# Kernel tuning notes

Hardware: AMD Instinct MI355X
Metric: run time of the kernel (lower is better)

## Reference

```python
import jax, jax.numpy as jnp
import numpy as np

B, L, D = 4, 1024, 256
HD = 16                 # head_dim
H = D // HD             # num heads = 16
DI = 2 * D              # mamba d_inner (expand=2) = 512
S = 64                  # d_state
KC = 4                  # d_conv
DTR = max(1, D // 16)   # dt_rank = 16
SCALES = (1, 2, 4, 8)


def _lin_interp(x, L_out):
    # F.interpolate(mode='linear', align_corners=False) on (B, L_in, D)
    L_in = x.shape[1]
    pos = (jnp.arange(L_out, dtype=x.dtype) + 0.5) * (L_in / L_out) - 0.5
    pos = jnp.clip(pos, 0.0, L_in - 1)
    lo = jnp.floor(pos).astype(jnp.int32)
    hi = jnp.minimum(lo + 1, L_in - 1)
    w = (pos - lo.astype(x.dtype))[None, :, None]
    return x[:, lo] * (1.0 - w) + x[:, hi] * w


def setup_inputs() -> dict:
    key = jax.random.key(0)
    ks = jax.random.split(key, 24)
    sc = 0.02
    inp = {
        "x": jax.random.normal(ks[0], (B, L, D), jnp.float32),
        "ln_g": jnp.ones((D,), jnp.float32),
        "ln_b": jnp.zeros((D,), jnp.float32),
        # MultiScaleQuery: 4 per-scale projections + fuse
        "mq_w": sc * jax.random.normal(ks[1], (4, D, D), jnp.float32),
        "mq_b": sc * jax.random.normal(ks[2], (4, D), jnp.float32),
        "fuse_w": sc * jax.random.normal(ks[3], (D, 4 * D), jnp.float32),
        "fuse_b": sc * jax.random.normal(ks[4], (D,), jnp.float32),
        # Mamba params
        "in_proj_w": sc * jax.random.normal(ks[5], (2 * DI, D), jnp.float32),
        "conv_w": 0.2 * jax.random.normal(ks[6], (DI, KC), jnp.float32),
        "conv_b": sc * jax.random.normal(ks[7], (DI,), jnp.float32),
        "x_proj_w": sc * jax.random.normal(ks[8], (DTR + 2 * S, DI), jnp.float32),
        "dt_w": sc * jax.random.normal(ks[9], (DI, DTR), jnp.float32),
        "dt_b": jnp.full((DI,), -4.0, jnp.float32),  # softplus -> small dt
        "A_log": jnp.log(jnp.tile(jnp.arange(1, S + 1, dtype=jnp.float32), (DI, 1))),
        "D_ssm": jnp.ones((DI,), jnp.float32),
        "out_w": sc * jax.random.normal(ks[10], (D, DI), jnp.float32),
        # StructuredSSD (q comes from MultiScaleQuery override; q_proj unused)
        "k_w": sc * jax.random.normal(ks[11], (D, D), jnp.float32),
        "k_b": sc * jax.random.normal(ks[12], (D,), jnp.float32),
        "v_w": sc * jax.random.normal(ks[13], (D, D), jnp.float32),
        "v_b": sc * jax.random.normal(ks[14], (D,), jnp.float32),
        "o_w": sc * jax.random.normal(ks[15], (D, D), jnp.float32),
        "o_b": sc * jax.random.normal(ks[16], (D,), jnp.float32),
        "log_tau": jnp.full((H,), np.log(16.0), jnp.float32),
        # Gate
        "gate_w": sc * jax.random.normal(ks[17], (D, 2 * D), jnp.float32),
        "gate_b": sc * jax.random.normal(ks[18], (D,), jnp.float32),
    }
    return inp


def reference(x, ln_g, ln_b, mq_w, mq_b, fuse_w, fuse_b,
              in_proj_w, conv_w, conv_b, x_proj_w, dt_w, dt_b,
              A_log, D_ssm, out_w,
              k_w, k_b, v_w, v_b, o_w, o_b, log_tau,
              gate_w, gate_b):
    Bsz, Lq, Dm = x.shape

    # ---- LayerNorm ----
    mu = x.mean(-1, keepdims=True)
    var = ((x - mu) ** 2).mean(-1, keepdims=True)
    xn = (x - mu) / jnp.sqrt(var + 1e-5) * ln_g + ln_b

    # ---- MultiScaleQuery ----
    qs = []
    for i, s in enumerate(SCALES):
        if s <= 1:
            q = xn @ mq_w[i].T + mq_b[i]
        else:
            xd = xn.reshape(Bsz, Lq // s, s, Dm).mean(2)   # avg_pool1d(k=s, stride=s)
            qd = xd @ mq_w[i].T + mq_b[i]
            q = _lin_interp(qd, Lq)
        qs.append(q)
    q = jnp.concatenate(qs, -1) @ fuse_w.T + fuse_b        # (B, L, D)

    # ---- Mamba (selective scan) ----
    xz = xn @ in_proj_w.T                                  # (B, L, 2*DI)
    xm, z = jnp.split(xz, 2, axis=-1)
    xp = jnp.pad(xm, ((0, 0), (KC - 1, 0), (0, 0)))        # causal depthwise conv
    xc = sum(xp[:, kk:kk + Lq, :] * conv_w[:, kk] for kk in range(KC)) + conv_b
    xc = jax.nn.silu(xc)                                   # (B, L, DI)
    dbc = xc @ x_proj_w.T                                  # (B, L, DTR+2S)
    dt_in, Bm, Cm = jnp.split(dbc, [DTR, DTR + S], axis=-1)
    dt = jax.nn.softplus(dt_in @ dt_w.T + dt_b)            # (B, L, DI)
    A = -jnp.exp(A_log)                                    # (DI, S)

    def step(h, inp):
        xt, dtt, Bt, Ct = inp                              # (B,DI) (B,DI) (B,S) (B,S)
        dA = jnp.exp(dtt[:, :, None] * A)                  # (B, DI, S)
        h = dA * h + (dtt * xt)[:, :, None] * Bt[:, None, :]
        y = jnp.einsum('bds,bs->bd', h, Ct)
        return h, y

    h0 = jnp.zeros((Bsz, DI, S), x.dtype)
    _, ys = jax.lax.scan(step, h0, (xc.transpose(1, 0, 2), dt.transpose(1, 0, 2),
                                    Bm.transpose(1, 0, 2), Cm.transpose(1, 0, 2)))
    y = ys.transpose(1, 0, 2) + xc * D_ssm                 # (B, L, DI)
    y = y * jax.nn.silu(z)
    ssm_out = y @ out_w.T                                  # (B, L, D)

    # ---- StructuredSSD (decay-masked attention, q override) ----
    k = xn @ k_w.T + k_b
    v = xn @ v_w.T + v_b
    hds = lambda t: t.reshape(Bsz, Lq, H, HD).transpose(0, 2, 1, 3)
    qh, kh, vh = hds(q), hds(k), hds(v)                    # (B, H, L, hd)
    scale = 1.0 / np.sqrt(HD)
    scores = jnp.einsum('bhqd,bhkd->bhqk', qh, kh) * scale
    idx = jnp.arange(Lq)
    dist = jnp.maximum(idx[:, None] - idx[None, :], 0).astype(x.dtype)
    tau = jnp.exp(log_tau)[:, None, None]                  # (H,1,1)
    mask = jnp.exp(-dist / tau)                            # (H, L, L); ==1 above diag
    scores = scores * mask
    denom = jnp.maximum(mask.sum(-1, keepdims=True), 1e-6)
    scores = scores / denom                                # broadcast over batch
    attn = jnp.einsum('bhqk,bhkd->bhqd', scores, vh)
    attn = attn.transpose(0, 2, 1, 3).reshape(Bsz, Lq, Dm)
    ssd_out = attn @ o_w.T + o_b

    # ---- Sigmoid gate fusion + residual ----
    gate = jax.nn.sigmoid(jnp.concatenate([ssm_out, ssd_out], -1) @ gate_w.T + gate_b)
    fused = gate * ssm_out + (1.0 - gate) * ssd_out
    return x + fused
```

## Files before the change

kernel.cpp:

```cpp
#include <hip/hip_runtime.h>
#include <math.h>

#define Bsz 4
#define Lseq 1024
#define Dm 256
#define Hh 16
#define HDm 16
#define DIm 512
#define Ssz 64
#define KCm 4
#define DTRm 16
#define NCH (Bsz * DIm)
#define CHK 64
#define NCHK (Lseq / CHK)
#define CHA 16
#define NCA (Lseq / CHA)

typedef __attribute__((ext_vector_type(8))) short s8v;
typedef __attribute__((ext_vector_type(4))) short s4v;
typedef __attribute__((ext_vector_type(4))) float f4v;
typedef unsigned short u16;

static __device__ __forceinline__ float wave_sum(float v) {
    #pragma unroll
    for (int m = 32; m >= 1; m >>= 1) v += __shfl_xor(v, m, 64);
    return v;
}

static __device__ __forceinline__ float bcast(float v, int l) {
    return __uint_as_float(__builtin_amdgcn_readlane(__float_as_uint(v), l));
}

static __device__ __forceinline__ short f2bf(float f) {
    unsigned int u = __float_as_uint(f);
    u = (u + 0x7fffu + ((u >> 16) & 1u)) >> 16;
    return (short)u;
}

static __device__ __forceinline__ float bf2f(u16 u) {
    return __uint_as_float(((unsigned int)u) << 16);
}

static __device__ __forceinline__ s8v pack8(float4 a, float4 b) {
    s8v v;
    v[0] = f2bf(a.x); v[1] = f2bf(a.y); v[2] = f2bf(a.z); v[3] = f2bf(a.w);
    v[4] = f2bf(b.x); v[5] = f2bf(b.y); v[6] = f2bf(b.z); v[7] = f2bf(b.w);
    return v;
}

static __device__ __forceinline__ s4v pack4(float4 a) {
    s4v v;
    v[0] = f2bf(a.x); v[1] = f2bf(a.y); v[2] = f2bf(a.z); v[3] = f2bf(a.w);
    return v;
}

__global__ __launch_bounds__(256) void ln_pool(const float* __restrict__ x,
                                               const float* __restrict__ g,
                                               const float* __restrict__ bb,
                                               u16* __restrict__ xnb, u16* __restrict__ xd2b,
                                               u16* __restrict__ xd4b, u16* __restrict__ xd8b,
                                               const float* __restrict__ in_proj_w,
                                               const float* __restrict__ k_w,
                                               const float* __restrict__ v_w,
                                               const float* __restrict__ mq_w,
                                               const float* __restrict__ fuse_w,
                                               const float* __restrict__ x_proj_w,
                                               const float* __restrict__ out_w,
                                               const float* __restrict__ o_w,
                                               const float* __restrict__ gate_w,
                                               u16* __restrict__ wbf) {
    int bx = blockIdx.x;
    int tid = threadIdx.x;
    if (bx < 512) {
        __shared__ float p2[4][256];
        int wid = tid >> 6, lane = tid & 63;
        int gr0 = bx * 8;
        int b = gr0 >> 10, t0 = gr0 & 1023;
        float4 g4 = *(const float4*)(g + lane * 4);
        float4 b4 = *(const float4*)(bb + lane * 4);
        float4 res[2];
        #pragma unroll
        for (int rr = 0; rr < 2; rr++) {
            int row = gr0 + wid * 2 + rr;
            float4 xv = *(const float4*)(x + (size_t)row * 256 + lane * 4);
            float s = wave_sum(xv.x + xv.y + xv.z + xv.w);
            float mean = s * (1.0f / 256.0f);
            float d0 = xv.x - mean, d1 = xv.y - mean, d2 = xv.z - mean, d3 = xv.w - mean;
            float s2 = wave_sum(d0 * d0 + d1 * d1 + d2 * d2 + d3 * d3);
            float inv = rsqrtf(s2 * (1.0f / 256.0f) + 1e-5f);
            float4 r;
            r.x = d0 * inv * g4.x + b4.x; r.y = d1 * inv * g4.y + b4.y;
            r.z = d2 * inv * g4.z + b4.z; r.w = d3 * inv * g4.w + b4.w;
            *(s4v*)(xnb + (size_t)row * 256 + lane * 4) = pack4(r);
            res[rr] = r;
        }
        float4 a2;
        a2.x = 0.5f * (res[0].x + res[1].x); a2.y = 0.5f * (res[0].y + res[1].y);
        a2.z = 0.5f * (res[0].z + res[1].z); a2.w = 0.5f * (res[0].w + res[1].w);
        *(s4v*)(xd2b + (size_t)(b * 512 + (t0 >> 1) + wid) * 256 + lane * 4) = pack4(a2);
        *(float4*)&p2[wid][lane * 4] = a2;
        __syncthreads();
        if (wid < 2) {
            float4 u = *(const float4*)&p2[2 * wid][lane * 4];
            float4 w = *(const float4*)&p2[2 * wid + 1][lane * 4];
            float4 m;
            m.x = 0.5f * (u.x + w.x); m.y = 0.5f * (u.y + w.y);
            m.z = 0.5f * (u.z + w.z); m.w = 0.5f * (u.w + w.w);
            *(s4v*)(xd4b + (size_t)(b * 256 + (t0 >> 2) + wid) * 256 + lane * 4) = pack4(m);
        } else if (wid == 2) {
            float4 q0 = *(const float4*)&p2[0][lane * 4];
            float4 q1 = *(const float4*)&p2[1][lane * 4];
            float4 q2 = *(const float4*)&p2[2][lane * 4];
            float4 q3 = *(const float4*)&p2[3][lane * 4];
            float4 m;
            m.x = 0.25f * ((q0.x + q1.x) + (q2.x + q3.x));
            m.y = 0.25f * ((q0.y + q1.y) + (q2.y + q3.y));
            m.z = 0.25f * ((q0.z + q1.z) + (q2.z + q3.z));
            m.w = 0.25f * ((q0.w + q1.w) + (q2.w + q3.w));
            *(s4v*)(xd8b + (size_t)(b * 128 + (t0 >> 3)) * 256 + lane * 4) = pack4(m);
        }
    } else {
        int l = bx - 512;
        const float* src; u16* dst; int base;
        if (l < 128)      { src = in_proj_w; dst = wbf;           base = l; }
        else if (l < 160) { src = k_w;      dst = wbf + 262144;   base = l - 128; }
        else if (l < 192) { src = v_w;      dst = wbf + 327680;   base = l - 160; }
        else if (l < 320) { src = mq_w;     dst = wbf + 393216;   base = l - 192; }
        else if (l < 448) { src = fuse_w;   dst = wbf + 655360;   base = l - 320; }
        else if (l < 484) { src = x_proj_w; dst = wbf + 917504;   base = l - 448; }
        else if (l < 548) { src = out_w;    dst = wbf + 991232;   base = l - 484; }
        else if (l < 580) { src = o_w;      dst = wbf + 1122304;  base = l - 548; }
        else              { src = gate_w;   dst = wbf + 1187840;  base = l - 580; }
        int idx = base * 2048 + tid * 8;
        const float* sp = src + idx;
        *(s8v*)(dst + idx) = pack8(*(const float4*)sp, *(const float4*)(sp + 4));
    }
}

__global__ __launch_bounds__(256) void proj8(const u16* __restrict__ xnb,
                                             const u16* __restrict__ xd2b,
                                             const u16* __restrict__ xd4b,
                                             const u16* __restrict__ xd8b,
                                             const u16* __restrict__ wbf,
                                             const float* __restrict__ k_b,
                                             const float* __restrict__ v_b,
                                             const float* __restrict__ mq_b,
                                             u16* __restrict__ xmb, float* __restrict__ zT,
                                             float* __restrict__ kmat, float* __restrict__ vmat,
                                             u16* __restrict__ q0b, u16* __restrict__ qd2b,
                                             u16* __restrict__ qd4b, u16* __restrict__ qd8b) {
    __shared__ u16 As[64][40];
    __shared__ u16 Ws[64][40];
    int bx = blockIdx.x;
    const u16* A; const u16* W; const float* bias;
    float* Cf = nullptr; u16* Cb = nullptr;
    int ldc, transC = 0, n0, m0;
    if (bx < 512) {
        A = xnb; W = wbf; bias = nullptr; Cb = xmb; ldc = DIm;
        n0 = (bx & 7) * 64; m0 = (bx >> 3) * 64;
    } else if (bx < 1024) {
        int l = bx - 512;
        A = xnb; W = wbf + 131072; bias = nullptr; Cf = zT; ldc = Bsz * Lseq; transC = 1;
        n0 = (l & 7) * 64; m0 = (l >> 3) * 64;
    } else if (bx < 1280) {
        int l = bx - 1024;
        A = xnb; W = wbf + 262144; bias = k_b; Cf = kmat; ldc = Dm;
        n0 = (l & 3) * 64; m0 = (l >> 2) * 64;
    } else if (bx < 1536) {
        int l = bx - 1280;
        A = xnb; W = wbf + 327680; bias = v_b; Cf = vmat; ldc = Dm;
        n0 = (l & 3) * 64; m0 = (l >> 2) * 64;
    } else if (bx < 1792) {
        int l = bx - 1536;
        A = xnb; W = wbf + 393216; bias = mq_b; Cb = q0b; ldc = Dm;
        n0 = (l & 3) * 64; m0 = (l >> 2) * 64;
    } else if (bx < 1920) {
        int l = bx - 1792;
        A = xd2b; W = wbf + 393216 + 65536; bias = mq_b + 256; Cb = qd2b; ldc = Dm;
        n0 = (l & 3) * 64; m0 = (l >> 2) * 64;
    } else if (bx < 1984) {
        int l = bx - 1920;
        A = xd4b; W = wbf + 393216 + 131072; bias = mq_b + 512; Cb = qd4b; ldc = Dm;
        n0 = (l & 3) * 64; m0 = (l >> 2) * 64;
    } else {
        int l = bx - 1984;
        A = xd8b; W = wbf + 393216 + 196608; bias = mq_b + 768; Cb = qd8b; ldc = Dm;
        n0 = (l & 3) * 64; m0 = (l >> 2) * 64;
    }
    int tid = threadIdx.x;
    int wave = tid >> 6, lane = tid & 63;
    int quad = lane >> 4, r = lane & 15;
    int mo = (wave >> 1) * 32, no = (wave & 1) * 32;
    f4v acc[2][2];
    #pragma unroll
    for (int i = 0; i < 2; i++)
        #pragma unroll
        for (int j = 0; j < 2; j++) acc[i][j] = (f4v){0.f, 0.f, 0.f, 0.f};
    for (int k0 = 0; k0 < 256; k0 += 32) {
        {
            int m = tid >> 2, kk = (tid & 3) * 8;
            *(s8v*)&As[m][kk] = *(const s8v*)(A + (size_t)(m0 + m) * 256 + k0 + kk);
        }
        {
            int n = tid >> 2, kk = (tid & 3) * 8;
            *(s8v*)&Ws[n][kk] = *(const s8v*)(W + (size_t)(n0 + n) * 256 + k0 + kk);
        }
        __syncthreads();
        s8v af[2], bf[2];
        #pragma unroll
        for (int i = 0; i < 2; i++) af[i] = *(const s8v*)&As[mo + i * 16 + r][quad * 8];
        #pragma unroll
        for (int j = 0; j < 2; j++) bf[j] = *(const s8v*)&Ws[no + j * 16 + r][quad * 8];
        #pragma unroll
        for (int i = 0; i < 2; i++)
            #pragma unroll
            for (int j = 0; j < 2; j++)
                acc[i][j] = __builtin_amdgcn_mfma_f32_16x16x32_bf16(af[i], bf[j], acc[i][j], 0, 0, 0);
        __syncthreads();
    }
    #pragma unroll
    for (int i = 0; i < 2; i++)
        #pragma unroll
        for (int j = 0; j < 2; j++)
            #pragma unroll
            for (int reg = 0; reg < 4; reg++) {
                int m = m0 + mo + i * 16 + quad * 4 + reg;
                int n = n0 + no + j * 16 + r;
                float v = acc[i][j][reg];
                if (bias) v += bias[n];
                if (Cb) Cb[(size_t)m * ldc + n] = (u16)f2bf(v);
                else {
                    float* cp = transC ? (Cf + (size_t)n * ldc + m) : (Cf + (size_t)m * ldc + n);
                    *cp = v;
                }
            }
}

__global__ __launch_bounds__(256) void mid2(const u16* __restrict__ q0b,
                                            const u16* __restrict__ qd2b,
                                            const u16* __restrict__ qd4b,
                                            const u16* __restrict__ qd8b,
                                            const u16* __restrict__ w_fuse,
                                            const float* __restrict__ fuse_b,
                                            float* __restrict__ qbuf,
                                            const u16* __restrict__ xmb,
                                            const float* __restrict__ cw,
                                            const float* __restrict__ cb,
                                            u16* __restrict__ xcb, float* __restrict__ xcT) {
    __shared__ __align__(16) char smem[16640];
    int bx = blockIdx.x;
    int tid = threadIdx.x;
    if (bx < 256) {
        u16 (*As)[40] = (u16(*)[40])smem;
        u16 (*Ws)[40] = (u16(*)[40])(smem + 5120);
        int wave = tid >> 6, lane = tid & 63;
        int quad = lane >> 4, r = lane & 15;
        int n0 = (bx & 3) * 64, m0 = (bx >> 2) * 64;
        int mo = (wave >> 1) * 32, no = (wave & 1) * 32;
        f4v acc[2][2];
        #pragma unroll
        for (int i = 0; i < 2; i++)
            #pragma unroll
            for (int j = 0; j < 2; j++) acc[i][j] = (f4v){0.f, 0.f, 0.f, 0.f};
        for (int k0 = 0; k0 < 1024; k0 += 32) {
            {
                int m = tid >> 2, kk = (tid & 3) * 8;
                int kg = k0 + kk;
                int seg = kg >> 8, dcol = kg & 255;
                int mg = m0 + m;
                s8v pv;
                if (seg == 0) {
                    pv = *(const s8v*)(q0b + (size_t)mg * 256 + dcol);
                } else {
                    int t = mg & 1023, b = mg >> 10;
                    int Lin = 512 >> (seg - 1);
                    const u16* qd = (seg == 1) ? qd2b : (seg == 2) ? qd4b : qd8b;
                    float pos = (t + 0.5f) * ((float)Lin / 1024.0f) - 0.5f;
                    pos = fminf(fmaxf(pos, 0.0f), (float)(Lin - 1));
                    int lo = (int)floorf(pos);
                    int hi = min(lo + 1, Lin - 1);
                    float w = pos - (float)lo;
                    s8v lv = *(const s8v*)(qd + ((size_t)(b * Lin + lo)) * 256 + dcol);
                    s8v hv = *(const s8v*)(qd + ((size_t)(b * Lin + hi)) * 256 + dcol);
                    #pragma unroll
                    for (int i = 0; i < 8; i++) {
                        float lf = bf2f((u16)lv[i]), hf = bf2f((u16)hv[i]);
                        pv[i] = f2bf(lf + w * (hf - lf));
                    }
                }
                *(s8v*)&As[m][kk] = pv;
            }
            {
                int n = tid >> 2, kk = (tid & 3) * 8;
                *(s8v*)&Ws[n][kk] = *(const s8v*)(w_fuse + (size_t)(n0 + n) * 1024 + k0 + kk);
            }
            __syncthreads();
            s8v af[2], bf[2];
            #pragma unroll
            for (int i = 0; i < 2; i++) af[i] = *(const s8v*)&As[mo + i * 16 + r][quad * 8];
            #pragma unroll
            for (int j = 0; j < 2; j++) bf[j] = *(const s8v*)&Ws[no + j * 16 + r][quad * 8];
            #pragma unroll
            for (int i = 0; i < 2; i++)
                #pragma unroll
                for (int j = 0; j < 2; j++)
                    acc[i][j] = __builtin_amdgcn_mfma_f32_16x16x32_bf16(af[i], bf[j], acc[i][j], 0, 0, 0);
            __syncthreads();
        }
        #pragma unroll
        for (int i = 0; i < 2; i++)
            #pragma unroll
            for (int j = 0; j < 2; j++)
                #pragma unroll
                for (int reg = 0; reg < 4; reg++) {
                    int m = m0 + mo + i * 16 + quad * 4 + reg;
                    int n = n0 + no + j * 16 + r;
                    qbuf[(size_t)m * 256 + n] = acc[i][j][reg] + fuse_b[n];
                }
    } else {
        float (*tile)[65] = (float(*)[65])smem;
        int blk = bx - 256;
        int cblk = blk & 7;
        int tblk = (blk >> 3) & 15;
        int b = blk >> 7;
        int c0 = cblk * 64, t0 = tblk * 64;
        int cc = tid & 63;
        int tw = tid >> 6;
        int c = c0 + cc;
        float w0 = cw[c * 4 + 0], w1 = cw[c * 4 + 1], w2 = cw[c * 4 + 2], w3 = cw[c * 4 + 3];
        float bias = cb[c];
        #pragma unroll 4
        for (int i = 0; i < 16; i++) {
            int tl = tw * 16 + i;
            int t = t0 + tl;
            const u16* base = xmb + ((size_t)(b * Lseq + t)) * DIm + c;
            float acc = bias + bf2f(base[0]) * w3;
            if (t >= 3) {
                acc += bf2f(base[-3 * DIm]) * w0 + bf2f(base[-2 * DIm]) * w1 + bf2f(base[-1 * DIm]) * w2;
            } else {
                if (t >= 1) acc += bf2f(base[-1 * DIm]) * w2;
                if (t >= 2) acc += bf2f(base[-2 * DIm]) * w1;
            }
            float r = acc / (1.0f + __expf(-acc));
            xcb[((size_t)(b * Lseq + t)) * DIm + c] = (u16)f2bf(r);
            tile[tl][cc] = r;
        }
        __syncthreads();
        int tcol = tid & 63;
        int crow0 = tid >> 6;
        #pragma unroll 4
        for (int j = 0; j < 16; j++) {
            int crow = crow0 * 16 + j;
            xcT[((size_t)(c0 + crow)) * (Bsz * Lseq) + b * Lseq + t0 + tcol] = tile[tcol][crow];
        }
    }
}

__global__ __launch_bounds__(256) void xproj_ap1(const u16* __restrict__ xcb,
                                                 const u16* __restrict__ w_xp,
                                                 float* __restrict__ dbc,
                                                 const float* __restrict__ kmat,
                                                 const float* __restrict__ vmat,
                                                 const float* __restrict__ log_tau,
                                                 float* __restrict__ loc) {
    __shared__ __align__(16) char smem[10240];
    int bx = blockIdx.x;
    int tid = threadIdx.x;
    int wid = tid >> 6, lane = tid & 63;
    if (bx < 192) {
        u16 (*As)[40] = (u16(*)[40])smem;
        u16 (*Ws)[40] = (u16(*)[40])(smem + 5120);
        int quad = lane >> 4, r = lane & 15;
        int n0 = (bx % 3) * 64, m0 = (bx / 3) * 64;
        int mo = (wid >> 1) * 32, no = (wid & 1) * 32;
        f4v acc[2][2];
        #pragma unroll
        for (int i = 0; i < 2; i++)
            #pragma unroll
            for (int j = 0; j < 2; j++) acc[i][j] = (f4v){0.f, 0.f, 0.f, 0.f};
        for (int k0 = 0; k0 < 512; k0 += 32) {
            {
                int m = tid >> 2, kk = (tid & 3) * 8;
                *(s8v*)&As[m][kk] = *(const s8v*)(xcb + (size_t)(m0 + m) * 512 + k0 + kk);
            }
            {
                int n = tid >> 2, kk = (tid & 3) * 8;
                s8v pv;
                if (n0 + n < 144) pv = *(const s8v*)(w_xp + (size_t)(n0 + n) * 512 + k0 + kk);
                else pv = (s8v){0, 0, 0, 0, 0, 0, 0, 0};
                *(s8v*)&Ws[n][kk] = pv;
            }
            __syncthreads();
            s8v af[2], bf[2];
            #pragma unroll
            for (int i = 0; i < 2; i++) af[i] = *(const s8v*)&As[mo + i * 16 + r][quad * 8];
            #pragma unroll
            for (int j = 0; j < 2; j++) bf[j] = *(const s8v*)&Ws[no + j * 16 + r][quad * 8];
            #pragma unroll
            for (int i = 0; i < 2; i++)
                #pragma unroll
                for (int j = 0; j < 2; j++)
                    acc[i][j] = __builtin_amdgcn_mfma_f32_16x16x32_bf16(af[i], bf[j], acc[i][j], 0, 0, 0);
            __syncthreads();
        }
        #pragma unroll
        for (int i = 0; i < 2; i++)
            #pragma unroll
            for (int j = 0; j < 2; j++)
                #pragma unroll
                for (int reg = 0; reg < 4; reg++) {
                    int m = m0 + mo + i * 16 + quad * 4 + reg;
                    int n = n0 + no + j * 16 + r;
                    if (n >= 144) continue;
                    dbc[(size_t)m * 144 + n] = acc[i][j][reg];
                }
    } else {
        float (*Ksh)[CHA][20] = (float(*)[CHA][20])smem;
        float (*Vsh)[CHA][16] = (float(*)[CHA][16])(smem + 5120);
        int wv = (bx - 192) * 4 + wid;
        int bh = wv >> 6, c = wv & 63;
        int b = bh >> 4, h = bh & 15;
        float inv_tau = __expf(-log_tau[h]);
        float rdec = __expf(-inv_tau);
        int t0 = c * CHA;
        int row = lane >> 2, q4 = (lane & 3) * 4;
        const float* kp = kmat + ((size_t)(b * Lseq + t0 + row)) * Dm + h * HDm + q4;
        const float* vp = vmat + ((size_t)(b * Lseq + t0 + row)) * Dm + h * HDm + q4;
        *(float4*)&Ksh[wid][row][q4] = *(const float4*)kp;
        *(float4*)&Vsh[wid][row][q4] = *(const float4*)vp;
        int g = lane >> 4, cc = lane & 15;
        float4 U = {0.f, 0.f, 0.f, 0.f}, T = {0.f, 0.f, 0.f, 0.f};
        #pragma unroll
        for (int s = 0; s < CHA; s++) {
            float4 kf = *(const float4*)&Ksh[wid][s][4 * g];
            float vv = Vsh[wid][s][cc];
            float u0 = kf.x * vv, u1 = kf.y * vv, u2 = kf.z * vv, u3 = kf.w * vv;
            U.x += u0; U.y += u1; U.z += u2; U.w += u3;
            T.x = fmaf(rdec, T.x, u0); T.y = fmaf(rdec, T.y, u1);
            T.z = fmaf(rdec, T.z, u2); T.w = fmaf(rdec, T.w, u3);
        }
        float* op = loc + ((size_t)bh * NCA + c) * 512;
        *(float4*)(op + lane * 4) = U;
        *(float4*)(op + 256 + lane * 4) = T;
    }
}

__global__ __launch_bounds__(256) void dt_ap2(const float* __restrict__ dbc,
                                              const float* __restrict__ dt_w,
                                              const float* __restrict__ dt_b,
                                              float* __restrict__ dtmT,
                                              float* __restrict__ loc,
                                              const float* __restrict__ log_tau,
                                              float* __restrict__ kvtot) {
    __shared__ __align__(16) char smem[9216];
    int bx = blockIdx.x;
    int tid = threadIdx.x;
    if (bx < 512) {
        float (*As)[72] = (float(*)[72])smem;
        float (*Ws)[72] = (float(*)[72])(smem + 4608);
        int m0 = (bx >> 3) * 64, n0 = (bx & 7) * 64;
        int tx = tid & 15, ty = tid >> 4;
        float acc[4][4] = {};
        {
            int ml = tid >> 2, kl = (tid & 3) * 4;
            const float4 av = *(const float4*)(dbc + (size_t)(m0 + ml) * 144 + kl);
            As[kl + 0][ml] = av.x; As[kl + 1][ml] = av.y;
            As[kl + 2][ml] = av.z; As[kl + 3][ml] = av.w;
        }
        {
            int nl = tid >> 2, kl = (tid & 3) * 4;
            float4 wv = *(const float4*)(dt_w + (size_t)(n0 + nl) * 16 + kl);
            Ws[kl + 0][nl] = wv.x; Ws[kl + 1][nl] = wv.y;
            Ws[kl + 2][nl] = wv.z; Ws[kl + 3][nl] = wv.w;
        }
        __syncthreads();
        #pragma unroll
        for (int kk = 0; kk < 16; kk++) {
            float4 av = *(const float4*)&As[kk][ty * 4];
            float4 bv = *(const float4*)&Ws[kk][tx * 4];
            float a[4] = {av.x, av.y, av.z, av.w};
            float bbv[4] = {bv.x, bv.y, bv.z, bv.w};
            #pragma unroll
            for (int im = 0; im < 4; im++)
                #pragma unroll
                for (int in = 0; in < 4; in++)
                    acc[im][in] = fmaf(a[im], bbv[in], acc[im][in]);
        }
        #pragma unroll
        for (int in = 0; in < 4; in++) {
            int n = n0 + tx * 4 + in;
            #pragma unroll
            for (int im = 0; im < 4; im++) {
                int m = m0 + ty * 4 + im;
                float v = acc[im][in] + dt_b[n];
                v = fmaxf(v, 0.0f) + log1pf(expf(-fabsf(v)));
                dtmT[(size_t)n * (Bsz * Lseq) + m] = v;
            }
        }
    } else {
        int bh = bx - 512, e = tid;
        float inv_tau = __expf(-log_tau[bh & 15]);
        float rp = __expf(-(float)CHA * inv_tau);
        float* lp = loc + (size_t)bh * NCA * 512;
        float Ua = 0.f, Ta = 0.f;
        #pragma unroll 8
        for (int c = 0; c < NCA; c++) {
            float tu = lp[c * 512 + e];
            lp[c * 512 + e] = Ua;
            Ua += tu;
            float tt = lp[c * 512 + 256 + e];
            lp[c * 512 + 256 + e] = Ta;
            Ta = fmaf(rp, Ta, tt);
        }
        kvtot[bh * 256 + e] = Ua;
    }
}

__global__ __launch_bounds__(256) void sp1_ap3(const float* __restrict__ xcT,
                                               const float* __restrict__ dtmT,
                                               const float* __restrict__ dbc,
                                               const float* __restrict__ A_log,
                                               float* __restrict__ hloc,
                                               float* __restrict__ Pc,
                                               const float* __restrict__ q,
                                               const float* __restrict__ kmat,
                                               const float* __restrict__ vmat,
                                               const float* __restrict__ log_tau,
                                               const float* __restrict__ init,
                                               const float* __restrict__ kvtot,
                                               u16* __restrict__ attnb) {
    __shared__ __align__(16) char smem[18432];
    int bx = blockIdx.x;
    int tid = threadIdx.x;
    int wid = tid >> 6, lane = tid & 63;
    if (bx < 8192) {
        int wave = bx * 4 + wid;
        int ch = wave & (NCH - 1);
        int c  = wave >> 11;
        int b = ch >> 9, d = ch & (DIm - 1);
        float As = -__expf(A_log[d * Ssz + lane]);
        int base_m = b * Lseq + c * CHK;
        float dt_vec = dtmT[(size_t)d * (Bsz * Lseq) + base_m + lane];
        float x_vec  = xcT [(size_t)d * (Bsz * Lseq) + base_m + lane];
        float ux = dt_vec * x_vec;
        float S = dt_vec;
        #pragma unroll
        for (int m = 1; m < 64; m <<= 1) {
            float o = __shfl_up(S, m, 64);
            if (lane >= m) S += o;
        }
        float Stot = bcast(S, 63);
        const float* Bp = dbc + (size_t)base_m * 144 + DTRm + lane;
        float h0 = 0.f, h1 = 0.f, h2 = 0.f, h3 = 0.f;
        #pragma unroll 4
        for (int t = 0; t < CHK; t += 4) {
            float B0 = Bp[0], B1 = Bp[144], B2 = Bp[288], B3 = Bp[432];
            Bp += 576;
            float w0 = __expf(As * (Stot - bcast(S, t)))     * bcast(ux, t);
            float w1 = __expf(As * (Stot - bcast(S, t + 1))) * bcast(ux, t + 1);
            float w2 = __expf(As * (Stot - bcast(S, t + 2))) * bcast(ux, t + 2);
            float w3 = __expf(As * (Stot - bcast(S, t + 3))) * bcast(ux, t + 3);
            h0 = fmaf(w0, B0, h0); h1 = fmaf(w1, B1, h1);
            h2 = fmaf(w2, B2, h2); h3 = fmaf(w3, B3, h3);
        }
        size_t o = ((size_t)ch * NCHK + c) * Ssz + lane;
        hloc[o] = (h0 + h1) + (h2 + h3);
        Pc[o] = __expf(As * Stot);
    } else {
        float (*Ksh)[CHA][20] = (float(*)[CHA][20])smem;
        float (*Qsh)[CHA][20] = (float(*)[CHA][20])(smem + 5120);
        float (*Vsh)[CHA][16] = (float(*)[CHA][16])(smem + 10240);
        float (*Ysh)[CHA][16] = (float(*)[CHA][16])(smem + 14336);
        int wv = (bx - 8192) * 4 + wid;
        int bh = wv >> 6, c = wv & 63;
        int b = bh >> 4, h = bh & 15;
        float inv_tau = __expf(-log_tau[h]);
        float rdec = __expf(-inv_tau);
        int t0 = c * CHA;
        int row = lane >> 2, q4 = (lane & 3) * 4;
        const float* kp = kmat + ((size_t)(b * Lseq + t0 + row)) * Dm + h * HDm + q4;
        const float* vp = vmat + ((size_t)(b * Lseq + t0 + row)) * Dm + h * HDm + q4;
        const float* qp = q    + ((size_t)(b * Lseq + t0 + row)) * Dm + h * HDm + q4;
        *(float4*)&Ksh[wid][row][q4] = *(const float4*)kp;
        *(float4*)&Vsh[wid][row][q4] = *(const float4*)vp;
        *(float4*)&Qsh[wid][row][q4] = *(const float4*)qp;
        int g = lane >> 4, cc = lane & 15;
        size_t ibase = ((size_t)bh * NCA + c) * 512;
        float4 U  = *(const float4*)(init + ibase + lane * 4);
        float4 T  = *(const float4*)(init + ibase + 256 + lane * 4);
        float4 KV = *(const float4*)(kvtot + bh * 256 + lane * 4);
        float om = 1.0f - rdec;
        float geom = (om > 1e-8f) ? (1.0f - __expf(-inv_tau * (float)t0)) / om : (float)t0;
        #pragma unroll
        for (int s = 0; s < CHA; s++) {
            int i = t0 + s;
            geom = fmaf(geom, rdec, 1.0f);
            float4 kf = *(const float4*)&Ksh[wid][s][4 * g];
            float4 qf = *(const float4*)&Qsh[wid][s][4 * g];
            float vv = Vsh[wid][s][cc];
            float u0 = kf.x * vv, u1 = kf.y * vv, u2 = kf.z * vv, u3 = kf.w * vv;
            U.x += u0; U.y += u1; U.z += u2; U.w += u3;
            T.x = fmaf(rdec, T.x, u0); T.y = fmaf(rdec, T.y, u1);
            T.z = fmaf(rdec, T.z, u2); T.w = fmaf(rdec, T.w, u3);
            float p;
            p = qf.x * (KV.x - U.x + T.x);
            p = fmaf(qf.y, KV.y - U.y + T.y, p);
            p = fmaf(qf.z, KV.z - U.z + T.z, p);
            p = fmaf(qf.w, KV.w - U.w + T.w, p);
            p += __shfl_xor(p, 16, 64);
            p += __shfl_xor(p, 32, 64);
            float deno = fmaxf((float)(Lseq - 1 - i) + geom, 1e-6f);
            float yv = p * (0.25f / deno);
            if (lane < 16) Ysh[wid][s][lane] = yv;
        }
        float4 yv4 = *(const float4*)&Ysh[wid][row][q4];
        *(s4v*)(attnb + ((size_t)(b * Lseq + t0 + row)) * Dm + h * HDm + q4) = pack4(yv4);
    }
}

__global__ __launch_bounds__(256) void comb_ssd(float* __restrict__ hloc,
                                                const float* __restrict__ Pc,
                                                const u16* __restrict__ attnb,
                                                const u16* __restrict__ w_o,
                                                const float* __restrict__ o_b,
                                                u16* __restrict__ cat2b) {
    __shared__ u16 As[64][40];
    __shared__ u16 Ws[64][40];
    int bx = blockIdx.x;
    int tid = threadIdx.x;
    if (bx < 512) {
        int wave = bx * 4 + (tid >> 6);
        int lane = tid & 63;
        size_t base = (size_t)wave * NCHK * Ssz + lane;
        float H = 0.0f;
        #pragma unroll
        for (int c = 0; c < NCHK; c++) {
            size_t o = base + (size_t)c * Ssz;
            float p = Pc[o];
            float hl = hloc[o];
            hloc[o] = H;
            H = fmaf(p, H, hl);
        }
    } else {
        int l = bx - 512;
        int wave = tid >> 6, lane = tid & 63;
        int quad = lane >> 4, r = lane & 15;
        int n0 = (l & 3) * 64, m0 = (l >> 2) * 64;
        int mo = (wave >> 1) * 32, no = (wave & 1) * 32;
        f4v acc[2][2];
        #pragma unroll
        for (int i = 0; i < 2; i++)
            #pragma unroll
            for (int j = 0; j < 2; j++) acc[i][j] = (f4v){0.f, 0.f, 0.f, 0.f};
        for (int k0 = 0; k0 < 256; k0 += 32) {
            {
                int m = tid >> 2, kk = (tid & 3) * 8;
                *(s8v*)&As[m][kk] = *(const s8v*)(attnb + (size_t)(m0 + m) * 256 + k0 + kk);
            }
            {
                int n = tid >> 2, kk = (tid & 3) * 8;
                *(s8v*)&Ws[n][kk] = *(const s8v*)(w_o + (size_t)(n0 + n) * 256 + k0 + kk);
            }
            __syncthreads();
            s8v af[2], bf[2];
            #pragma unroll
            for (int i = 0; i < 2; i++) af[i] = *(const s8v*)&As[mo + i * 16 + r][quad * 8];
            #pragma unroll
            for (int j = 0; j < 2; j++) bf[j] = *(const s8v*)&Ws[no + j * 16 + r][quad * 8];
            #pragma unroll
            for (int i = 0; i < 2; i++)
                #pragma unroll
                for (int j = 0; j < 2; j++)
                    acc[i][j] = __builtin_amdgcn_mfma_f32_16x16x32_bf16(af[i], bf[j], acc[i][j], 0, 0, 0);
            __syncthreads();
        }
        #pragma unroll
        for (int i = 0; i < 2; i++)
            #pragma unroll
            for (int j = 0; j < 2; j++)
                #pragma unroll
                for (int reg = 0; reg < 4; reg++) {
                    int m = m0 + mo + i * 16 + quad * 4 + reg;
                    int n = n0 + no + j * 16 + r;
                    cat2b[(size_t)m * 512 + 256 + n] = (u16)f2bf(acc[i][j][reg] + o_b[n]);
                }
    }
}

__global__ __launch_bounds__(256) void scan_pass3(const float* __restrict__ xcT,
                                                  const float* __restrict__ dtmT,
                                                  const float* __restrict__ zT,
                                                  const float* __restrict__ dbc,
                                                  const float* __restrict__ A_log,
                                                  const float* __restrict__ D_ssm,
                                                  const float* __restrict__ Hinit,
                                                  u16* __restrict__ yTb) {
    __shared__ float hCs[4][16][68];
    int wid = threadIdx.x >> 6;
    int lane = threadIdx.x & 63;
    int wave = blockIdx.x * 4 + wid;
    int ch = wave & (NCH - 1);
    int c  = wave >> 11;
    int b = ch >> 9, d = ch & (DIm - 1);
    float As = -__expf(A_log[d * Ssz + lane]);
    float Dd = D_ssm[d];
    int base_m = b * Lseq + c * CHK;
    float dt_vec = dtmT[(size_t)d * (Bsz * Lseq) + base_m + lane];
    float x_vec  = xcT [(size_t)d * (Bsz * Lseq) + base_m + lane];
    float zown   = zT  [(size_t)d * (Bsz * Lseq) + base_m + lane];
    float ux = dt_vec * x_vec;
    const float* Bp = dbc + (size_t)base_m * 144 + DTRm + lane;
    const float* Cp = Bp + Ssz;
    float h = Hinit[((size_t)ch * NCHK + c) * Ssz + lane];
    float yred = 0.0f;
    int tl = lane >> 2;
    int so = (lane & 3) * 16;
    for (int tb = 0; tb < 4; tb++) {
        #pragma unroll
        for (int j = 0; j < 16; j++) {
            int t = tb * 16 + j;
            float Bt = *Bp; Bp += 144;
            float Ct = *Cp; Cp += 144;
            float dtv = bcast(dt_vec, t);
            float u   = bcast(ux, t);
            float dA = __expf(dtv * As);
            h = fmaf(dA, h, u * Bt);
            hCs[wid][j][lane] = h * Ct;
        }
        const float* bp = &hCs[wid][tl][so];
        float4 a0 = *(const float4*)(bp + 0);
        float4 a1 = *(const float4*)(bp + 4);
        float4 a2 = *(const float4*)(bp + 8);
        float4 a3 = *(const float4*)(bp + 12);
        float part = ((a0.x + a0.y) + (a0.z + a0.w)) + ((a1.x + a1.y) + (a1.z + a1.w))
                   + ((a2.x + a2.y) + (a2.z + a2.w)) + ((a3.x + a3.y) + (a3.z + a3.w));
        part += __shfl_xor(part, 1, 64);
        part += __shfl_xor(part, 2, 64);
        float got = __shfl(part, ((lane - tb * 16) << 2) & 63, 64);
        if ((lane >> 4) == tb) yred = got;
    }
    float yg = (yred + x_vec * Dd) * (zown / (1.0f + __expf(-zown)));
    yTb[(size_t)d * (Bsz * Lseq) + base_m + lane] = (u16)f2bf(yg);
}

__global__ __launch_bounds__(256) void outg(const u16* __restrict__ yTb,
                                            const u16* __restrict__ w_out,
                                            u16* __restrict__ cat2b) {
    __shared__ u16 As[64][40];
    __shared__ u16 Ws[64][40];
    int bx = blockIdx.x;
    int tid = threadIdx.x;
    int wave = tid >> 6, lane = tid & 63;
    int quad = lane >> 4, r = lane & 15;
    int n0 = (bx & 3) * 64, m0 = (bx >> 2) * 64;
    int mo = (wave >> 1) * 32, no = (wave & 1) * 32;
    f4v acc[2][2];
    #pragma unroll
    for (int i = 0; i < 2; i++)
        #pragma unroll
        for (int j = 0; j < 2; j++) acc[i][j] = (f4v){0.f, 0.f, 0.f, 0.f};
    for (int k0 = 0; k0 < 512; k0 += 32) {
        {
            int k = tid >> 3, m8 = (tid & 7) * 8;
            s8v av = *(const s8v*)(yTb + (size_t)(k0 + k) * (Bsz * Lseq) + m0 + m8);
            #pragma unroll
            for (int i = 0; i < 8; i++) As[m8 + i][k] = (u16)av[i];
        }
        {
            int n = tid >> 2, kk = (tid & 3) * 8;
            *(s8v*)&Ws[n][kk] = *(const s8v*)(w_out + (size_t)(n0 + n) * 512 + k0 + kk);
        }
        __syncthreads();
        s8v af[2], bf[2];
        #pragma unroll
        for (int i = 0; i < 2; i++) af[i] = *(const s8v*)&As[mo + i * 16 + r][quad * 8];
        #pragma unroll
        for (int j = 0; j < 2; j++) bf[j] = *(const s8v*)&Ws[no + j * 16 + r][quad * 8];
        #pragma unroll
        for (int i = 0; i < 2; i++)
            #pragma unroll
            for (int j = 0; j < 2; j++)
                acc[i][j] = __builtin_amdgcn_mfma_f32_16x16x32_bf16(af[i], bf[j], acc[i][j], 0, 0, 0);
        __syncthreads();
    }
    #pragma unroll
    for (int i = 0; i < 2; i++)
        #pragma unroll
        for (int j = 0; j < 2; j++)
            #pragma unroll
            for (int reg = 0; reg < 4; reg++) {
                int m = m0 + mo + i * 16 + quad * 4 + reg;
                int n = n0 + no + j * 16 + r;
                cat2b[(size_t)m * 512 + n] = (u16)f2bf(acc[i][j][reg]);
            }
}

__global__ __launch_bounds__(256) void gate_gemm(const u16* __restrict__ cat2b,
                                                 const u16* __restrict__ w_gate,
                                                 const float* __restrict__ gate_b,
                                                 const float* __restrict__ xres,
                                                 float* __restrict__ fout) {
    __shared__ u16 As[64][40];
    __shared__ u16 Ws[64][40];
    int tid = threadIdx.x;
    int wave = tid >> 6, lane = tid & 63;
    int quad = lane >> 4, r = lane & 15;
    int m0 = blockIdx.y * 64, n0 = blockIdx.x * 64;
    int mo = (wave >> 1) * 32, no = (wave & 1) * 32;
    f4v acc[2][2];
    #pragma unroll
    for (int i = 0; i < 2; i++)
        #pragma unroll
        for (int j = 0; j < 2; j++) acc[i][j] = (f4v){0.f, 0.f, 0.f, 0.f};
    for (int k0 = 0; k0 < 512; k0 += 32) {
        {
            int m = tid >> 2, kk = (tid & 3) * 8;
            *(s8v*)&As[m][kk] = *(const s8v*)(cat2b + (size_t)(m0 + m) * 512 + k0 + kk);
        }
        {
            int n = tid >> 2, kk = (tid & 3) * 8;
            *(s8v*)&Ws[n][kk] = *(const s8v*)(w_gate + (size_t)(n0 + n) * 512 + k0 + kk);
        }
        __syncthreads();
        s8v af[2], bf[2];
        #pragma unroll
        for (int i = 0; i < 2; i++) af[i] = *(const s8v*)&As[mo + i * 16 + r][quad * 8];
        #pragma unroll
        for (int j = 0; j < 2; j++) bf[j] = *(const s8v*)&Ws[no + j * 16 + r][quad * 8];
        #pragma unroll
        for (int i = 0; i < 2; i++)
            #pragma unroll
            for (int j = 0; j < 2; j++)
                acc[i][j] = __builtin_amdgcn_mfma_f32_16x16x32_bf16(af[i], bf[j], acc[i][j], 0, 0, 0);
        __syncthreads();
    }
    #pragma unroll
    for (int i = 0; i < 2; i++)
        #pragma unroll
        for (int j = 0; j < 2; j++)
            #pragma unroll
            for (int reg = 0; reg < 4; reg++) {
                int m = m0 + mo + i * 16 + quad * 4 + reg;
                int n = n0 + no + j * 16 + r;
                float v = acc[i][j][reg] + gate_b[n];
                float gg = 1.0f / (1.0f + __expf(-v));
                float ssm = bf2f(cat2b[(size_t)m * 512 + n]);
                float ssd = bf2f(cat2b[(size_t)m * 512 + 256 + n]);
                fout[(size_t)m * 256 + n] = xres[(size_t)m * 256 + n] + gg * ssm + (1.0f - gg) * ssd;
            }
}

extern "C" void kernel_launch(void* const* d_in, const int* in_sizes, int n_in,
                              void* d_out, int out_size, void* d_ws, size_t ws_size,
                              hipStream_t stream) {
    const float* x        = (const float*)d_in[0];
    const float* ln_g     = (const float*)d_in[1];
    const float* ln_b     = (const float*)d_in[2];
    const float* mq_w     = (const float*)d_in[3];
    const float* mq_b     = (const float*)d_in[4];
    const float* fuse_w   = (const float*)d_in[5];
    const float* fuse_b   = (const float*)d_in[6];
    const float* in_proj_w= (const float*)d_in[7];
    const float* conv_w   = (const float*)d_in[8];
    const float* conv_b   = (const float*)d_in[9];
    const float* x_proj_w = (const float*)d_in[10];
    const float* dt_w     = (const float*)d_in[11];
    const float* dt_b     = (const float*)d_in[12];
    const float* A_log    = (const float*)d_in[13];
    const float* D_ssm    = (const float*)d_in[14];
    const float* out_w    = (const float*)d_in[15];
    const float* k_w      = (const float*)d_in[16];
    const float* k_b      = (const float*)d_in[17];
    const float* v_w      = (const float*)d_in[18];
    const float* v_b      = (const float*)d_in[19];
    const float* o_w      = (const float*)d_in[20];
    const float* o_b      = (const float*)d_in[21];
    const float* log_tau  = (const float*)d_in[22];
    const float* gate_w   = (const float*)d_in[23];
    const float* gate_b   = (const float*)d_in[24];
    float* outp = (float*)d_out;

    const int M = Bsz * Lseq;
    float* ws = (float*)d_ws;
    size_t off = 0;
    float* zT    = ws + off; off += (size_t)DIm * M;
    float* xcT   = ws + off; off += (size_t)DIm * M;
    float* dtmT  = ws + off; off += (size_t)DIm * M;
    float* dbc   = ws + off; off += (size_t)M * 144;
    float* qbuf  = ws + off; off += (size_t)M * Dm;
    float* kmat  = ws + off; off += (size_t)M * Dm;
    float* vmat  = ws + off; off += (size_t)M * Dm;
    float* loc   = ws + off; off += (size_t)64 * NCA * 512;
    float* hloc  = ws + off; off += (size_t)NCH * NCHK * Ssz;
    float* Pc    = ws + off; off += (size_t)NCH * NCHK * Ssz;
    float* kvtot = ws + off; off += (size_t)64 * 256;
    u16* ub = (u16*)(ws + off);
    size_t uo = 0;
    u16* xnb  = ub + uo; uo += (size_t)M * Dm;
    u16* xmb  = ub + uo; uo += (size_t)M * DIm;
    u16* xd2b = ub + uo; uo += (size_t)2048 * Dm;
    u16* xd4b = ub + uo; uo += (size_t)1024 * Dm;
    u16* xd8b = ub + uo; uo += (size_t)512 * Dm;
    u16* q0b  = ub + uo; uo += (size_t)M * Dm;
    u16* qd2b = ub + uo; uo += (size_t)2048 * Dm;
    u16* qd4b = ub + uo; uo += (size_t)1024 * Dm;
    u16* qd8b = ub + uo; uo += (size_t)512 * Dm;
    u16* attnb= ub + uo; uo += (size_t)M * Dm;
    u16* cat2b= ub + uo; uo += (size_t)M * 2 * Dm;
    u16* yTb  = ub + uo; uo += (size_t)DIm * M;
    u16* wbf  = ub + uo; uo += 1318912;
    u16* xcb  = cat2b;

    ln_pool<<<1156, 256, 0, stream>>>(x, ln_g, ln_b, xnb, xd2b, xd4b, xd8b,
        in_proj_w, k_w, v_w, mq_w, fuse_w, x_proj_w, out_w, o_w, gate_w, wbf);

    proj8<<<2016, 256, 0, stream>>>(xnb, xd2b, xd4b, xd8b, wbf,
        k_b, v_b, mq_b, xmb, zT, kmat, vmat, q0b, qd2b, qd4b, qd8b);

    mid2<<<768, 256, 0, stream>>>(q0b, qd2b, qd4b, qd8b, wbf + 655360, fuse_b, qbuf,
        xmb, conv_w, conv_b, xcb, xcT);

    xproj_ap1<<<1216, 256, 0, stream>>>(xcb, wbf + 917504, dbc, kmat, vmat, log_tau, loc);

    dt_ap2<<<576, 256, 0, stream>>>(dbc, dt_w, dt_b, dtmT, loc, log_tau, kvtot);

    sp1_ap3<<<9216, 256, 0, stream>>>(xcT, dtmT, dbc, A_log, hloc, Pc,
        qbuf, kmat, vmat, log_tau, loc, kvtot, attnb);

    comb_ssd<<<768, 256, 0, stream>>>(hloc, Pc, attnb, wbf + 1122304, o_b, cat2b);

    scan_pass3<<<8192, 256, 0, stream>>>(xcT, dtmT, zT, dbc, A_log, D_ssm, hloc, yTb);

    outg<<<256, 256, 0, stream>>>(yTb, wbf + 991232, cat2b);

    gate_gemm<<<dim3(4, 64), 256, 0, stream>>>(cat2b, wbf + 1187840, gate_b, x, outp);
}
```

Before: 294.2 us.

## Fold dt projection into weights and restructure kernel chain with precomputed gate weights

Precomputes the combined dt_w·x_proj weight and the product of the gate weight with the out-projection weight in the prep kernel. dt is then computed directly by one bf16 MFMA GEMM with fused softplus, and the gate pre-activation is split into two GEMM partial sums plus a separate elementwise final kernel. Stages are regrouped into fewer, differently fused launches (sp1_ap2, comb_ap3, p3_og, outg_gpre, final_k), and a shared MFMA core helper replaces the duplicated loops. The aim is fewer launches and less fp32 dt work. The cost is extra bf16 rounding of the folded weights and additional fp32 intermediate buffers.

```diff
diff --git a/kernel.cpp b/kernel.cpp
--- a/kernel.cpp
+++ b/kernel.cpp
@@ -8,13 +8,13 @@
 #define HDm 16
 #define DIm 512
 #define Ssz 64
-#define KCm 4
 #define DTRm 16
 #define NCH (Bsz * DIm)
 #define CHK 64
 #define NCHK (Lseq / CHK)
 #define CHA 16
 #define NCA (Lseq / CHA)
+#define LOG2E 1.44269504088896f
 
 typedef __attribute__((ext_vector_type(8))) short s8v;
 typedef __attribute__((ext_vector_type(4))) short s4v;
@@ -53,6 +53,51 @@
     v[0] = f2bf(a.x); v[1] = f2bf(a.y); v[2] = f2bf(a.z); v[3] = f2bf(a.w);
     return v;
 }
+
+static __device__ __forceinline__ void mfma_core(const u16* __restrict__ A, int lda,
+                                                 const u16* __restrict__ W, int ldw,
+                                                 int m0, int n0, int K,
+                                                 u16 (*As)[40], u16 (*Ws)[40],
+                                                 f4v acc[2][2], int tid) {
+    int wave = tid >> 6, lane = tid & 63;
+    int quad = lane >> 4, r = lane & 15;
+    int mo = (wave >> 1) * 32, no = (wave & 1) * 32;
+    for (int k0 = 0; k0 < K; k0 += 32) {
+        {
+            int m = tid >> 2, kk = (tid & 3) * 8;
+            *(s8v*)&As[m][kk] = *(const s8v*)(A + (size_t)(m0 + m) * lda + k0 + kk);
+        }
+        {
+            int n = tid >> 2, kk = (tid & 3) * 8;
+            *(s8v*)&Ws[n][kk] = *(const s8v*)(W + (size_t)(n0 + n) * ldw + k0 + kk);
+        }
+        __syncthreads();
+        s8v af[2], bf[2];
+        #pragma unroll
+        for (int i = 0; i < 2; i++) af[i] = *(const s8v*)&As[mo + i * 16 + r][quad * 8];
+        #pragma unroll
+        for (int j = 0; j < 2; j++) bf[j] = *(const s8v*)&Ws[no + j * 16 + r][quad * 8];
+        #pragma unroll
+        for (int i = 0; i < 2; i++)
+            #pragma unroll
+            for (int j = 0; j < 2; j++)
+                acc[i][j] = __builtin_amdgcn_mfma_f32_16x16x32_bf16(af[i], bf[j], acc[i][j], 0, 0, 0);
+        __syncthreads();
+    }
+}
+
+#define WB_INPJ 0
+#define WB_K    262144
+#define WB_V    327680
+#define WB_MQ   393216
+#define WB_FUSE 655360
+#define WB_XP   917504
+#define WB_OUT  991232
+#define WB_O    1122304
+#define WB_GATE 1187840
+#define WB_OUTT 1318912
+#define WB_WDT  1449984
+#define WB_W1P  1712128
 
 __global__ __launch_bounds__(256) void ln_pool(const float* __restrict__ x,
                                                const float* __restrict__ g,
@@ -68,6 +113,7 @@
                                                const float* __restrict__ out_w,
                                                const float* __restrict__ o_w,
                                                const float* __restrict__ gate_w,
+                                               const float* __restrict__ dt_w,
                                                u16* __restrict__ wbf) {
     int bx = blockIdx.x;
     int tid = threadIdx.x;
@@ -119,21 +165,44 @@
             m.w = 0.25f * ((q0.w + q1.w) + (q2.w + q3.w));
             *(s4v*)(xd8b + (size_t)(b * 128 + (t0 >> 3)) * 256 + lane * 4) = pack4(m);
         }
-    } else {
+    } else if (bx < 1156) {
         int l = bx - 512;
         const float* src; u16* dst; int base;
-        if (l < 128)      { src = in_proj_w; dst = wbf;           base = l; }
-        else if (l < 160) { src = k_w;      dst = wbf + 262144;   base = l - 128; }
-        else if (l < 192) { src = v_w;      dst = wbf + 327680;   base = l - 160; }
-        else if (l < 320) { src = mq_w;     dst = wbf + 393216;   base = l - 192; }
-        else if (l < 448) { src = fuse_w;   dst = wbf + 655360;   base = l - 320; }
-        else if (l < 484) { src = x_proj_w; dst = wbf + 917504;   base = l - 448; }
-        else if (l < 548) { src = out_w;    dst = wbf + 991232;   base = l - 484; }
-        else if (l < 580) { src = o_w;      dst = wbf + 1122304;  base = l - 548; }
-        else              { src = gate_w;   dst = wbf + 1187840;  base = l - 580; }
+        if (l < 128)      { src = in_proj_w; dst = wbf + WB_INPJ; base = l; }
+        else if (l < 160) { src = k_w;      dst = wbf + WB_K;    base = l - 128; }
+        else if (l < 192) { src = v_w;      dst = wbf + WB_V;    base = l - 160; }
+        else if (l < 320) { src = mq_w;     dst = wbf + WB_MQ;   base = l - 192; }
+        else if (l < 448) { src = fuse_w;   dst = wbf + WB_FUSE; base = l - 320; }
+        else if (l < 484) { src = x_proj_w; dst = wbf + WB_XP;   base = l - 448; }
+        else if (l < 548) { src = out_w;    dst = wbf + WB_OUT;  base = l - 484; }
+        else if (l < 580) { src = o_w;      dst = wbf + WB_O;    base = l - 548; }
+        else              { src = gate_w;   dst = wbf + WB_GATE; base = l - 580; }
         int idx = base * 2048 + tid * 8;
         const float* sp = src + idx;
         *(s8v*)(dst + idx) = pack8(*(const float4*)sp, *(const float4*)(sp + 4));
+    } else if (bx < 1412) {
+        int l = bx - 1156;
+        int gid = l * 1024 + tid * 4;
+        int n = gid >> 9, d0 = gid & 511;
+        float4 acc = {0.f, 0.f, 0.f, 0.f};
+        #pragma unroll
+        for (int k = 0; k < 16; k++) {
+            float wv = dt_w[n * 16 + k];
+            float4 xp = *(const float4*)(x_proj_w + (size_t)k * 512 + d0);
+            acc.x = fmaf(wv, xp.x, acc.x); acc.y = fmaf(wv, xp.y, acc.y);
+            acc.z = fmaf(wv, xp.z, acc.z); acc.w = fmaf(wv, xp.w, acc.w);
+        }
+        *(s4v*)(wbf + WB_WDT + (size_t)n * 512 + d0) = pack4(acc);
+    } else {
+        int l = bx - 1412;
+        int gid = l * 2048 + tid * 8;
+        int k = gid >> 9, d0 = gid & 511;
+        float4 a0 = *(const float4*)(out_w + (size_t)k * 512 + d0);
+        float4 a1 = *(const float4*)(out_w + (size_t)k * 512 + d0 + 4);
+        float vv[8] = {a0.x, a0.y, a0.z, a0.w, a1.x, a1.y, a1.z, a1.w};
+        #pragma unroll
+        for (int i = 0; i < 8; i++)
+            wbf[WB_OUTT + (size_t)(d0 + i) * 256 + k] = (u16)f2bf(vv[i]);
     }
 }
 
@@ -141,7 +210,7 @@
                                              const u16* __restrict__ xd2b,
                                              const u16* __restrict__ xd4b,
                                              const u16* __restrict__ xd8b,
-                                             const u16* __restrict__ wbf,
+                                             u16* __restrict__ wbf,
                                              const float* __restrict__ k_b,
                                              const float* __restrict__ v_b,
                                              const float* __restrict__ mq_b,
@@ -152,72 +221,59 @@
     __shared__ u16 As[64][40];
     __shared__ u16 Ws[64][40];
     int bx = blockIdx.x;
+    int tid = threadIdx.x;
     const u16* A; const u16* W; const float* bias;
     float* Cf = nullptr; u16* Cb = nullptr;
-    int ldc, transC = 0, n0, m0;
+    int lda, ldw, ldc, K = 256, n0, m0;
     if (bx < 512) {
-        A = xnb; W = wbf; bias = nullptr; Cb = xmb; ldc = DIm;
+        A = xnb; lda = 256; W = wbf + WB_INPJ; ldw = 256; bias = nullptr; Cb = xmb; ldc = DIm;
         n0 = (bx & 7) * 64; m0 = (bx >> 3) * 64;
     } else if (bx < 1024) {
         int l = bx - 512;
-        A = xnb; W = wbf + 131072; bias = nullptr; Cf = zT; ldc = Bsz * Lseq; transC = 1;
-        n0 = (l & 7) * 64; m0 = (l >> 3) * 64;
+        A = wbf + WB_INPJ + 131072; lda = 256; W = xnb; ldw = 256; bias = nullptr;
+        Cf = zT; ldc = 4096;
+        m0 = (l >> 6) * 64; n0 = (l & 63) * 64;
     } else if (bx < 1280) {
         int l = bx - 1024;
-        A = xnb; W = wbf + 262144; bias = k_b; Cf = kmat; ldc = Dm;
+        A = xnb; lda = 256; W = wbf + WB_K; ldw = 256; bias = k_b; Cf = kmat; ldc = Dm;
         n0 = (l & 3) * 64; m0 = (l >> 2) * 64;
     } else if (bx < 1536) {
         int l = bx - 1280;
-        A = xnb; W = wbf + 327680; bias = v_b; Cf = vmat; ldc = Dm;
+        A = xnb; lda = 256; W = wbf + WB_V; ldw = 256; bias = v_b; Cf = vmat; ldc = Dm;
         n0 = (l & 3) * 64; m0 = (l >> 2) * 64;
     } else if (bx < 1792) {
         int l = bx - 1536;
-        A = xnb; W = wbf + 393216; bias = mq_b; Cb = q0b; ldc = Dm;
+        A = xnb; lda = 256; W = wbf + WB_MQ; ldw = 256; bias = mq_b; Cb = q0b; ldc = Dm;
         n0 = (l & 3) * 64; m0 = (l >> 2) * 64;
     } else if (bx < 1920) {
         int l = bx - 1792;
-        A = xd2b; W = wbf + 393216 + 65536; bias = mq_b + 256; Cb = qd2b; ldc = Dm;
+        A = xd2b; lda = 256; W = wbf + WB_MQ + 65536; ldw = 256; bias = mq_b + 256; Cb = qd2b; ldc = Dm;
         n0 = (l & 3) * 64; m0 = (l >> 2) * 64;
     } else if (bx < 1984) {
         int l = bx - 1920;
-        A = xd4b; W = wbf + 393216 + 131072; bias = mq_b + 512; Cb = qd4b; ldc = Dm;
+        A = xd4b; lda = 256; W = wbf + WB_MQ + 131072; ldw = 256; bias = mq_b + 512; Cb = qd4b; ldc = Dm;
         n0 = (l & 3) * 64; m0 = (l >> 2) * 64;
     } else {
-        int l = bx - 1984;
-        A = xd8b; W = wbf + 393216 + 196608; bias = mq_b + 768; Cb = qd8b; ldc = Dm;
-        n0 = (l & 3) * 64; m0 = (l >> 2) * 64;
+        if (bx < 2016) {
+            int l = bx - 1984;
+            A = xd8b; lda = 256; W = wbf + WB_MQ + 196608; ldw = 256; bias = mq_b + 768; Cb = qd8b; ldc = Dm;
+            n0 = (l & 3) * 64; m0 = (l >> 2) * 64;
+        } else {
+            int l = bx - 2016;
+            A = wbf + WB_GATE; lda = 512; W = wbf + WB_OUTT; ldw = 256; bias = nullptr;
+            Cb = wbf + WB_W1P; ldc = 512;
+            m0 = (l >> 3) * 64; n0 = (l & 7) * 64;
+        }
     }
-    int tid = threadIdx.x;
+    f4v acc[2][2];
+    #pragma unroll
+    for (int i = 0; i < 2; i++)
+        #pragma unroll
+        for (int j = 0; j < 2; j++) acc[i][j] = (f4v){0.f, 0.f, 0.f, 0.f};
+    mfma_core(A, lda, W, ldw, m0, n0, K, As, Ws, acc, tid);
     int wave = tid >> 6, lane = tid & 63;
     int quad = lane >> 4, r = lane & 15;
     int mo = (wave >> 1) * 32, no = (wave & 1) * 32;
-    f4v acc[2][2];
-    #pragma unroll
-    for (int i = 0; i < 2; i++)
-        #pragma unroll
-        for (int j = 0; j < 2; j++) acc[i][j] = (f4v){0.f, 0.f, 0.f, 0.f};
-    for (int k0 = 0; k0 < 256; k0 += 32) {
-        {
-            int m = tid >> 2, kk = (tid & 3) * 8;
-            *(s8v*)&As[m][kk] = *(const s8v*)(A + (size_t)(m0 + m) * 256 + k0 + kk);
-        }
-        {
-            int n = tid >> 2, kk = (tid & 3) * 8;
-            *(s8v*)&Ws[n][kk] = *(const s8v*)(W + (size_t)(n0 + n) * 256 + k0 + kk);
-        }
-        __syncthreads();
-        s8v af[2], bf[2];
-        #pragma unroll
-        for (int i = 0; i < 2; i++) af[i] = *(const s8v*)&As[mo + i * 16 + r][quad * 8];
-        #pragma unroll
-        for (int j = 0; j < 2; j++) bf[j] = *(const s8v*)&Ws[no + j * 16 + r][quad * 8];
-        #pragma unroll
-        for (int i = 0; i < 2; i++)
-            #pragma unroll
-            for (int j = 0; j < 2; j++)
-                acc[i][j] = __builtin_amdgcn_mfma_f32_16x16x32_bf16(af[i], bf[j], acc[i][j], 0, 0, 0);
-        __syncthreads();
-    }
     #pragma unroll
     for (int i = 0; i < 2; i++)
         #pragma unroll
@@ -229,10 +285,7 @@
                 float v = acc[i][j][reg];
                 if (bias) v += bias[n];
                 if (Cb) Cb[(size_t)m * ldc + n] = (u16)f2bf(v);
-                else {
-                    float* cp = transC ? (Cf + (size_t)n * ldc + m) : (Cf + (size_t)m * ldc + n);
-                    *cp = v;
-                }
+                else Cf[(size_t)m * ldc + n] = v;
             }
 }
 
@@ -357,8 +410,10 @@
 }
 
 __global__ __launch_bounds__(256) void xproj_ap1(const u16* __restrict__ xcb,
-                                                 const u16* __restrict__ w_xp,
-                                                 float* __restrict__ dbc,
+                                                 const u16* __restrict__ wbf,
+                                                 float* __restrict__ dbc2,
+                                                 const float* __restrict__ dt_b,
+                                                 float* __restrict__ dtmT,
                                                  const float* __restrict__ kmat,
                                                  const float* __restrict__ vmat,
                                                  const float* __restrict__ log_tau,
@@ -367,42 +422,27 @@
     int bx = blockIdx.x;
     int tid = threadIdx.x;
     int wid = tid >> 6, lane = tid & 63;
-    if (bx < 192) {
+    if (bx < 640) {
         u16 (*As)[40] = (u16(*)[40])smem;
         u16 (*Ws)[40] = (u16(*)[40])(smem + 5120);
+        const u16* A; const u16* W;
+        int lda, ldw, K, m0, n0, mode;
+        if (bx < 128) {
+            A = xcb; lda = 512; W = wbf + WB_XP + 16 * 512; ldw = 512; K = 512;
+            n0 = (bx & 1) * 64; m0 = (bx >> 1) * 64; mode = 0;
+        } else {
+            int l = bx - 128;
+            A = wbf + WB_WDT; lda = 512; W = xcb; ldw = 512; K = 512;
+            m0 = (l >> 6) * 64; n0 = (l & 63) * 64; mode = 1;
+        }
+        f4v acc[2][2];
+        #pragma unroll
+        for (int i = 0; i < 2; i++)
+            #pragma unroll
+            for (int j = 0; j < 2; j++) acc[i][j] = (f4v){0.f, 0.f, 0.f, 0.f};
+        mfma_core(A, lda, W, ldw, m0, n0, K, As, Ws, acc, tid);
         int quad = lane >> 4, r = lane & 15;
-        int n0 = (bx % 3) * 64, m0 = (bx / 3) * 64;
         int mo = (wid >> 1) * 32, no = (wid & 1) * 32;
-        f4v acc[2][2];
-        #pragma unroll
-        for (int i = 0; i < 2; i++)
-            #pragma unroll
-            for (int j = 0; j < 2; j++) acc[i][j] = (f4v){0.f, 0.f, 0.f, 0.f};
-        for (int k0 = 0; k0 < 512; k0 += 32) {
-            {
-                int m = tid >> 2, kk = (tid & 3) * 8;
-                *(s8v*)&As[m][kk] = *(const s8v*)(xcb + (size_t)(m0 + m) * 512 + k0 + kk);
-            }
-            {
-                int n = tid >> 2, kk = (tid & 3) * 8;
-                s8v pv;
-                if (n0 + n < 144) pv = *(const s8v*)(w_xp + (size_t)(n0 + n) * 512 + k0 + kk);
-                else pv = (s8v){0, 0, 0, 0, 0, 0, 0, 0};
-                *(s8v*)&Ws[n][kk] = pv;
-            }
-            __syncthreads();
-            s8v af[2], bf[2];
-            #pragma unroll
-            for (int i = 0; i < 2; i++) af[i] = *(const s8v*)&As[mo + i * 16 + r][quad * 8];
-            #pragma unroll
-            for (int j = 0; j < 2; j++) bf[j] = *(const s8v*)&Ws[no + j * 16 + r][quad * 8];
-            #pragma unroll
-            for (int i = 0; i < 2; i++)
-                #pragma unroll
-                for (int j = 0; j < 2; j++)
-                    acc[i][j] = __builtin_amdgcn_mfma_f32_16x16x32_bf16(af[i], bf[j], acc[i][j], 0, 0, 0);
-            __syncthreads();
-        }
         #pragma unroll
         for (int i = 0; i < 2; i++)
             #pragma unroll
@@ -411,13 +451,19 @@
                 for (int reg = 0; reg < 4; reg++) {
                     int m = m0 + mo + i * 16 + quad * 4 + reg;
                     int n = n0 + no + j * 16 + r;
-                    if (n >= 144) continue;
-                    dbc[(size_t)m * 144 + n] = acc[i][j][reg];
+                    float v = acc[i][j][reg];
+                    if (mode == 0) {
+                        dbc2[(size_t)m * 128 + n] = v;
+                    } else {
+                        v += dt_b[m];
+                        v = fmaxf(v, 0.0f) + log1pf(__expf(-fabsf(v)));
+                        dtmT[(size_t)m * 4096 + n] = v;
+                    }
                 }
     } else {
         float (*Ksh)[CHA][20] = (float(*)[CHA][20])smem;
         float (*Vsh)[CHA][16] = (float(*)[CHA][16])(smem + 5120);
-        int wv = (bx - 192) * 4 + wid;
+        int wv = (bx - 640) * 4 + wid;
         int bh = wv >> 6, c = wv & 63;
         int b = bh >> 4, h = bh & 15;
         float inv_tau = __expf(-log_tau[h]);
@@ -445,60 +491,53 @@
     }
 }
 
-__global__ __launch_bounds__(256) void dt_ap2(const float* __restrict__ dbc,
-                                              const float* __restrict__ dt_w,
-                                              const float* __restrict__ dt_b,
-                                              float* __restrict__ dtmT,
-                                              float* __restrict__ loc,
-                                              const float* __restrict__ log_tau,
-                                              float* __restrict__ kvtot) {
-    __shared__ __align__(16) char smem[9216];
+__global__ __launch_bounds__(256) void sp1_ap2(const float* __restrict__ xcT,
+                                               const float* __restrict__ dtmT,
+                                               const float* __restrict__ dbc2,
+                                               const float* __restrict__ A_log,
+                                               float* __restrict__ hloc,
+                                               float* __restrict__ Pc,
+                                               float* __restrict__ loc,
+                                               const float* __restrict__ log_tau,
+                                               float* __restrict__ kvtot) {
     int bx = blockIdx.x;
     int tid = threadIdx.x;
-    if (bx < 512) {
-        float (*As)[72] = (float(*)[72])smem;
-        float (*Ws)[72] = (float(*)[72])(smem + 4608);
-        int m0 = (bx >> 3) * 64, n0 = (bx & 7) * 64;
-        int tx = tid & 15, ty = tid >> 4;
-        float acc[4][4] = {};
-        {
-            int ml = tid >> 2, kl = (tid & 3) * 4;
-            const float4 av = *(const float4*)(dbc + (size_t)(m0 + ml) * 144 + kl);
-            As[kl + 0][ml] = av.x; As[kl + 1][ml] = av.y;
-            As[kl + 2][ml] = av.z; As[kl + 3][ml] = av.w;
-        }
-        {
-            int nl = tid >> 2, kl = (tid & 3) * 4;
-            float4 wv = *(const float4*)(dt_w + (size_t)(n0 + nl) * 16 + kl);
-            Ws[kl + 0][nl] = wv.x; Ws[kl + 1][nl] = wv.y;
-            Ws[kl + 2][nl] = wv.z; Ws[kl + 3][nl] = wv.w;
-        }
-        __syncthreads();
-        #pragma unroll
-        for (int kk = 0; kk < 16; kk++) {
-            float4 av = *(const float4*)&As[kk][ty * 4];
-            float4 bv = *(const float4*)&Ws[kk][tx * 4];
-            float a[4] = {av.x, av.y, av.z, av.w};
-            float bbv[4] = {bv.x, bv.y, bv.z, bv.w};
-            #pragma unroll
-            for (int im = 0; im < 4; im++)
-                #pragma unroll
-                for (int in = 0; in < 4; in++)
-                    acc[im][in] = fmaf(a[im], bbv[in], acc[im][in]);
-        }
-        #pragma unroll
-        for (int in = 0; in < 4; in++) {
-            int n = n0 + tx * 4 + in;
-            #pragma unroll
-            for (int im = 0; im < 4; im++) {
-                int m = m0 + ty * 4 + im;
-                float v = acc[im][in] + dt_b[n];
-                v = fmaxf(v, 0.0f) + log1pf(expf(-fabsf(v)));
-                dtmT[(size_t)n * (Bsz * Lseq) + m] = v;
-            }
-        }
+    int wid = tid >> 6, lane = tid & 63;
+    if (bx < 8192) {
+        int wave = bx * 4 + wid;
+        int ch = wave & (NCH - 1);
+        int c  = wave >> 11;
+        int b = ch >> 9, d = ch & (DIm - 1);
+        float As2 = -__expf(A_log[d * Ssz + lane]) * LOG2E;
+        int base_m = b * Lseq + c * CHK;
+        float dt_vec = dtmT[(size_t)d * (Bsz * Lseq) + base_m + lane];
+        float x_vec  = xcT [(size_t)d * (Bsz * Lseq) + base_m + lane];
+        float ux = dt_vec * x_vec;
+        float S = dt_vec;
+        #pragma unroll
+        for (int m = 1; m < 64; m <<= 1) {
+            float o = __shfl_up(S, m, 64);
+            if (lane >= m) S += o;
+        }
+        float Stot = bcast(S, 63);
+        const float* Bp = dbc2 + (size_t)base_m * 128 + lane;
+        float h0 = 0.f, h1 = 0.f, h2 = 0.f, h3 = 0.f;
+        #pragma unroll 4
+        for (int t = 0; t < CHK; t += 4) {
+            float B0 = Bp[0], B1 = Bp[128], B2 = Bp[256], B3 = Bp[384];
+            Bp += 512;
+            float w0 = exp2f(As2 * (Stot - bcast(S, t)))     * bcast(ux, t);
+            float w1 = exp2f(As2 * (Stot - bcast(S, t + 1))) * bcast(ux, t + 1);
+            float w2 = exp2f(As2 * (Stot - bcast(S, t + 2))) * bcast(ux, t + 2);
+            float w3 = exp2f(As2 * (Stot - bcast(S, t + 3))) * bcast(ux, t + 3);
+            h0 = fmaf(w0, B0, h0); h1 = fmaf(w1, B1, h1);
+            h2 = fmaf(w2, B2, h2); h3 = fmaf(w3, B3, h3);
+        }
+        size_t o = ((size_t)ch * NCHK + c) * Ssz + lane;
+        hloc[o] = (h0 + h1) + (h2 + h3);
+        Pc[o] = exp2f(As2 * Stot);
     } else {
-        int bh = bx - 512, e = tid;
+        int bh = bx - 8192, e = tid;
         float inv_tau = __expf(-log_tau[bh & 15]);
         float rp = __expf(-(float)CHA * inv_tau);
         float* lp = loc + (size_t)bh * NCA * 512;
@@ -516,62 +555,37 @@
     }
 }
 
-__global__ __launch_bounds__(256) void sp1_ap3(const float* __restrict__ xcT,
-                                               const float* __restrict__ dtmT,
-                                               const float* __restrict__ dbc,
-                                               const float* __restrict__ A_log,
-                                               float* __restrict__ hloc,
-                                               float* __restrict__ Pc,
-                                               const float* __restrict__ q,
-                                               const float* __restrict__ kmat,
-                                               const float* __restrict__ vmat,
-                                               const float* __restrict__ log_tau,
-                                               const float* __restrict__ init,
-                                               const float* __restrict__ kvtot,
-                                               u16* __restrict__ attnb) {
+__global__ __launch_bounds__(256) void comb_ap3(float* __restrict__ hloc,
+                                                const float* __restrict__ Pc,
+                                                const float* __restrict__ q,
+                                                const float* __restrict__ kmat,
+                                                const float* __restrict__ vmat,
+                                                const float* __restrict__ log_tau,
+                                                const float* __restrict__ init,
+                                                const float* __restrict__ kvtot,
+                                                u16* __restrict__ attnb) {
     __shared__ __align__(16) char smem[18432];
     int bx = blockIdx.x;
     int tid = threadIdx.x;
     int wid = tid >> 6, lane = tid & 63;
-    if (bx < 8192) {
+    if (bx < 512) {
         int wave = bx * 4 + wid;
-        int ch = wave & (NCH - 1);
-        int c  = wave >> 11;
-        int b = ch >> 9, d = ch & (DIm - 1);
-        float As = -__expf(A_log[d * Ssz + lane]);
-        int base_m = b * Lseq + c * CHK;
-        float dt_vec = dtmT[(size_t)d * (Bsz * Lseq) + base_m + lane];
-        float x_vec  = xcT [(size_t)d * (Bsz * Lseq) + base_m + lane];
-        float ux = dt_vec * x_vec;
-        float S = dt_vec;
-        #pragma unroll
-        for (int m = 1; m < 64; m <<= 1) {
-            float o = __shfl_up(S, m, 64);
-            if (lane >= m) S += o;
-        }
-        float Stot = bcast(S, 63);
-        const float* Bp = dbc + (size_t)base_m * 144 + DTRm + lane;
-        float h0 = 0.f, h1 = 0.f, h2 = 0.f, h3 = 0.f;
-        #pragma unroll 4
-        for (int t = 0; t < CHK; t += 4) {
-            float B0 = Bp[0], B1 = Bp[144], B2 = Bp[288], B3 = Bp[432];
-            Bp += 576;
-            float w0 = __expf(As * (Stot - bcast(S, t)))     * bcast(ux, t);
-            float w1 = __expf(As * (Stot - bcast(S, t + 1))) * bcast(ux, t + 1);
-            float w2 = __expf(As * (Stot - bcast(S, t + 2))) * bcast(ux, t + 2);
-            float w3 = __expf(As * (Stot - bcast(S, t + 3))) * bcast(ux, t + 3);
-            h0 = fmaf(w0, B0, h0); h1 = fmaf(w1, B1, h1);
-            h2 = fmaf(w2, B2, h2); h3 = fmaf(w3, B3, h3);
-        }
-        size_t o = ((size_t)ch * NCHK + c) * Ssz + lane;
-        hloc[o] = (h0 + h1) + (h2 + h3);
-        Pc[o] = __expf(As * Stot);
+        size_t base = (size_t)wave * NCHK * Ssz + lane;
+        float H = 0.0f;
+        #pragma unroll
+        for (int c = 0; c < NCHK; c++) {
+            size_t o = base + (size_t)c * Ssz;
+            float p = Pc[o];
+            float hl = hloc[o];
+            hloc[o] = H;
+            H = fmaf(p, H, hl);
+        }
     } else {
         float (*Ksh)[CHA][20] = (float(*)[CHA][20])smem;
         float (*Qsh)[CHA][20] = (float(*)[CHA][20])(smem + 5120);
         float (*Vsh)[CHA][16] = (float(*)[CHA][16])(smem + 10240);
         float (*Ysh)[CHA][16] = (float(*)[CHA][16])(smem + 14336);
-        int wv = (bx - 8192) * 4 + wid;
+        int wv = (bx - 512) * 4 + wid;
         int bh = wv >> 6, c = wv & 63;
         int b = bh >> 4, h = bh & 15;
         float inv_tau = __expf(-log_tau[h]);
@@ -618,62 +632,80 @@
     }
 }
 
-__global__ __launch_bounds__(256) void comb_ssd(float* __restrict__ hloc,
-                                                const float* __restrict__ Pc,
-                                                const u16* __restrict__ attnb,
-                                                const u16* __restrict__ w_o,
-                                                const float* __restrict__ o_b,
-                                                u16* __restrict__ cat2b) {
-    __shared__ u16 As[64][40];
-    __shared__ u16 Ws[64][40];
+__global__ __launch_bounds__(256) void p3_og(const float* __restrict__ xcT,
+                                             const float* __restrict__ dtmT,
+                                             const float* __restrict__ zT,
+                                             const float* __restrict__ dbc2,
+                                             const float* __restrict__ A_log,
+                                             const float* __restrict__ D_ssm,
+                                             const float* __restrict__ Hinit,
+                                             u16* __restrict__ yTb,
+                                             const u16* __restrict__ attnb,
+                                             const u16* __restrict__ w_o,
+                                             const float* __restrict__ o_b,
+                                             u16* __restrict__ cat2b) {
+    __shared__ __align__(16) char smem[17408];
     int bx = blockIdx.x;
     int tid = threadIdx.x;
-    if (bx < 512) {
-        int wave = bx * 4 + (tid >> 6);
-        int lane = tid & 63;
-        size_t base = (size_t)wave * NCHK * Ssz + lane;
-        float H = 0.0f;
-        #pragma unroll
-        for (int c = 0; c < NCHK; c++) {
-            size_t o = base + (size_t)c * Ssz;
-            float p = Pc[o];
-            float hl = hloc[o];
-            hloc[o] = H;
-            H = fmaf(p, H, hl);
-        }
+    int wid = tid >> 6, lane = tid & 63;
+    if (bx < 8192) {
+        float (*hCs)[16][68] = (float(*)[16][68])smem;
+        int wave = bx * 4 + wid;
+        int ch = wave & (NCH - 1);
+        int c  = wave >> 11;
+        int b = ch >> 9, d = ch & (DIm - 1);
+        float As2 = -__expf(A_log[d * Ssz + lane]) * LOG2E;
+        float Dd = D_ssm[d];
+        int base_m = b * Lseq + c * CHK;
+        float dt_vec = dtmT[(size_t)d * (Bsz * Lseq) + base_m + lane];
+        float x_vec  = xcT [(size_t)d * (Bsz * Lseq) + base_m + lane];
+        float zown   = zT  [(size_t)d * (Bsz * Lseq) + base_m + lane];
+        float ux = dt_vec * x_vec;
+        const float* Bp = dbc2 + (size_t)base_m * 128 + lane;
+        const float* Cp = Bp + 64;
+        float h = Hinit[((size_t)ch * NCHK + c) * Ssz + lane];
+        float yred = 0.0f;
+        int tl = lane >> 2;
+        int so = (lane & 3) * 16;
+        for (int tb = 0; tb < 4; tb++) {
+            #pragma unroll
+            for (int j = 0; j < 16; j++) {
+                int t = tb * 16 + j;
+                float Bt = *Bp; Bp += 128;
+                float Ct = *Cp; Cp += 128;
+                float dtv = bcast(dt_vec, t);
+                float u   = bcast(ux, t);
+                float dA = exp2f(As2 * dtv);
+                h = fmaf(dA, h, u * Bt);
+                hCs[wid][j][lane] = h * Ct;
+            }
+            const float* bp = &hCs[wid][tl][so];
+            float4 a0 = *(const float4*)(bp + 0);
+            float4 a1 = *(const float4*)(bp + 4);
+            float4 a2 = *(const float4*)(bp + 8);
+            float4 a3 = *(const float4*)(bp + 12);
+            float part = ((a0.x + a0.y) + (a0.z + a0.w)) + ((a1.x + a1.y) + (a1.z + a1.w))
+                       + ((a2.x + a2.y) + (a2.z + a2.w)) + ((a3.x + a3.y) + (a3.z + a3.w));
+            part += __shfl_xor(part, 1, 64);
+            part += __shfl_xor(part, 2, 64);
+            float got = __shfl(part, ((lane - tb * 16) << 2) & 63, 64);
+            if ((lane >> 4) == tb) yred = got;
+        }
+        float yg = (yred + x_vec * Dd) * (zown / (1.0f + __expf(-zown)));
+        yTb[(size_t)d * (Bsz * Lseq) + base_m + lane] = (u16)f2bf(yg);
     } else {
-        int l = bx - 512;
-        int wave = tid >> 6, lane = tid & 63;
+        u16 (*As)[40] = (u16(*)[40])smem;
+        u16 (*Ws)[40] = (u16(*)[40])(smem + 5120);
+        int l = bx - 8192;
+        int n0 = (l & 3) * 64, m0 = (l >> 2) * 64;
+        f4v acc[2][2];
+        #pragma unroll
+        for (int i = 0; i < 2; i++)
+            #pragma unroll
+            for (int j = 0; j < 2; j++) acc[i][j] = (f4v){0.f, 0.f, 0.f, 0.f};
+        mfma_core(attnb, 256, w_o, 256, m0, n0, 256, As, Ws, acc, tid);
         int quad = lane >> 4, r = lane & 15;
-        int n0 = (l & 3) * 64, m0 = (l >> 2) * 64;
-        int mo = (wave >> 1) * 32, no = (wave & 1) * 32;
-        f4v acc[2][2];
-        #pragma unroll
-        for (int i = 0; i < 2; i++)
-            #pragma unroll
-            for (int j = 0; j < 2; j++) acc[i][j] = (f4v){0.f, 0.f, 0.f, 0.f};
-        for (int k0 = 0; k0 < 256; k0 += 32) {
-            {
-                int m = tid >> 2, kk = (tid & 3) * 8;
-                *(s8v*)&As[m][kk] = *(const s8v*)(attnb + (size_t)(m0 + m) * 256 + k0 + kk);
-            }
-            {
-                int n = tid >> 2, kk = (tid & 3) * 8;
-                *(s8v*)&Ws[n][kk] = *(const s8v*)(w_o + (size_t)(n0 + n) * 256 + k0 + kk);
-            }
-            __syncthreads();
-            s8v af[2], bf[2];
-            #pragma unroll
-            for (int i = 0; i < 2; i++) af[i] = *(const s8v*)&As[mo + i * 16 + r][quad * 8];
-            #pragma unroll
-            for (int j = 0; j < 2; j++) bf[j] = *(const s8v*)&Ws[no + j * 16 + r][quad * 8];
-            #pragma unroll
-            for (int i = 0; i < 2; i++)
-                #pragma unroll
-                for (int j = 0; j < 2; j++)
-                    acc[i][j] = __builtin_amdgcn_mfma_f32_16x16x32_bf16(af[i], bf[j], acc[i][j], 0, 0, 0);
-            __syncthreads();
-        }
+        int mo = (wid >> 1) * 32, no = (wid & 1) * 32;
         #pragma unroll
         for (int i = 0; i < 2; i++)
             #pragma unroll
@@ -687,167 +719,108 @@
     }
 }
 
-__global__ __launch_bounds__(256) void scan_pass3(const float* __restrict__ xcT,
-                                                  const float* __restrict__ dtmT,
-                                                  const float* __restrict__ zT,
-                                                  const float* __restrict__ dbc,
-                                                  const float* __restrict__ A_log,
-                                                  const float* __restrict__ D_ssm,
-                                                  const float* __restrict__ Hinit,
-                                                  u16* __restrict__ yTb) {
-    __shared__ float hCs[4][16][68];
-    int wid = threadIdx.x >> 6;
-    int lane = threadIdx.x & 63;
-    int wave = blockIdx.x * 4 + wid;
-    int ch = wave & (NCH - 1);
-    int c  = wave >> 11;
-    int b = ch >> 9, d = ch & (DIm - 1);
-    float As = -__expf(A_log[d * Ssz + lane]);
-    float Dd = D_ssm[d];
-    int base_m = b * Lseq + c * CHK;
-    float dt_vec = dtmT[(size_t)d * (Bsz * Lseq) + base_m + lane];
-    float x_vec  = xcT [(size_t)d * (Bsz * Lseq) + base_m + lane];
-    float zown   = zT  [(size_t)d * (Bsz * Lseq) + base_m + lane];
-    float ux = dt_vec * x_vec;
-    const float* Bp = dbc + (size_t)base_m * 144 + DTRm + lane;
-    const float* Cp = Bp + Ssz;
-    float h = Hinit[((size_t)ch * NCHK + c) * Ssz + lane];
-    float yred = 0.0f;
-    int tl = lane >> 2;
-    int so = (lane & 3) * 16;
-    for (int tb = 0; tb < 4; tb++) {
-        #pragma unroll
-        for (int j = 0; j < 16; j++) {
-            int t = tb * 16 + j;
-            float Bt = *Bp; Bp += 144;
-            float Ct = *Cp; Cp += 144;
-            float dtv = bcast(dt_vec, t);
-            float u   = bcast(ux, t);
-            float dA = __expf(dtv * As);
-            h = fmaf(dA, h, u * Bt);
-            hCs[wid][j][lane] = h * Ct;
-        }
-        const float* bp = &hCs[wid][tl][so];
-        float4 a0 = *(const float4*)(bp + 0);
-        float4 a1 = *(const float4*)(bp + 4);
-        float4 a2 = *(const float4*)(bp + 8);
-        float4 a3 = *(const float4*)(bp + 12);
-        float part = ((a0.x + a0.y) + (a0.z + a0.w)) + ((a1.x + a1.y) + (a1.z + a1.w))
-                   + ((a2.x + a2.y) + (a2.z + a2.w)) + ((a3.x + a3.y) + (a3.z + a3.w));
-        part += __shfl_xor(part, 1, 64);
-        part += __shfl_xor(part, 2, 64);
-        float got = __shfl(part, ((lane - tb * 16) << 2) & 63, 64);
-        if ((lane >> 4) == tb) yred = got;
-    }
-    float yg = (yred + x_vec * Dd) * (zown / (1.0f + __expf(-zown)));
-    yTb[(size_t)d * (Bsz * Lseq) + base_m + lane] = (u16)f2bf(yg);
-}
-
-__global__ __launch_bounds__(256) void outg(const u16* __restrict__ yTb,
-                                            const u16* __restrict__ w_out,
-                                            u16* __restrict__ cat2b) {
+__global__ __launch_bounds__(256) void outg_gpre(const u16* __restrict__ yTb,
+                                                 const u16* __restrict__ wbf,
+                                                 const u16* __restrict__ cat2b_ssd,
+                                                 u16* __restrict__ cat2b,
+                                                 float* __restrict__ gpre1,
+                                                 float* __restrict__ gpre2) {
     __shared__ u16 As[64][40];
     __shared__ u16 Ws[64][40];
     int bx = blockIdx.x;
     int tid = threadIdx.x;
     int wave = tid >> 6, lane = tid & 63;
     int quad = lane >> 4, r = lane & 15;
-    int n0 = (bx & 3) * 64, m0 = (bx >> 2) * 64;
     int mo = (wave >> 1) * 32, no = (wave & 1) * 32;
     f4v acc[2][2];
     #pragma unroll
     for (int i = 0; i < 2; i++)
         #pragma unroll
         for (int j = 0; j < 2; j++) acc[i][j] = (f4v){0.f, 0.f, 0.f, 0.f};
-    for (int k0 = 0; k0 < 512; k0 += 32) {
-        {
-            int k = tid >> 3, m8 = (tid & 7) * 8;
-            s8v av = *(const s8v*)(yTb + (size_t)(k0 + k) * (Bsz * Lseq) + m0 + m8);
-            #pragma unroll
-            for (int i = 0; i < 8; i++) As[m8 + i][k] = (u16)av[i];
-        }
-        {
-            int n = tid >> 2, kk = (tid & 3) * 8;
-            *(s8v*)&Ws[n][kk] = *(const s8v*)(w_out + (size_t)(n0 + n) * 512 + k0 + kk);
-        }
-        __syncthreads();
-        s8v af[2], bf[2];
-        #pragma unroll
-        for (int i = 0; i < 2; i++) af[i] = *(const s8v*)&As[mo + i * 16 + r][quad * 8];
-        #pragma unroll
-        for (int j = 0; j < 2; j++) bf[j] = *(const s8v*)&Ws[no + j * 16 + r][quad * 8];
+    if (bx < 512) {
+        int mode = bx >> 8;
+        int l = bx & 255;
+        int n0 = (l & 3) * 64, m0 = (l >> 2) * 64;
+        const u16* W = mode ? (wbf + WB_W1P) : (wbf + WB_OUT);
+        for (int k0 = 0; k0 < 512; k0 += 32) {
+            {
+                int k = tid >> 3, m8 = (tid & 7) * 8;
+                s8v av = *(const s8v*)(yTb + (size_t)(k0 + k) * (Bsz * Lseq) + m0 + m8);
+                #pragma unroll
+                for (int i = 0; i < 8; i++) As[m8 + i][k] = (u16)av[i];
+            }
+            {
+                int n = tid >> 2, kk = (tid & 3) * 8;
+                *(s8v*)&Ws[n][kk] = *(const s8v*)(W + (size_t)(n0 + n) * 512 + k0 + kk);
+            }
+            __syncthreads();
+            s8v af[2], bf[2];
+            #pragma unroll
+            for (int i = 0; i < 2; i++) af[i] = *(const s8v*)&As[mo + i * 16 + r][quad * 8];
+            #pragma unroll
+            for (int j = 0; j < 2; j++) bf[j] = *(const s8v*)&Ws[no + j * 16 + r][quad * 8];
+            #pragma unroll
+            for (int i = 0; i < 2; i++)
+                #pragma unroll
+                for (int j = 0; j < 2; j++)
+                    acc[i][j] = __builtin_amdgcn_mfma_f32_16x16x32_bf16(af[i], bf[j], acc[i][j], 0, 0, 0);
+            __syncthreads();
+        }
         #pragma unroll
         for (int i = 0; i < 2; i++)
             #pragma unroll
             for (int j = 0; j < 2; j++)
-                acc[i][j] = __builtin_amdgcn_mfma_f32_16x16x32_bf16(af[i], bf[j], acc[i][j], 0, 0, 0);
-        __syncthreads();
+                #pragma unroll
+                for (int reg = 0; reg < 4; reg++) {
+                    int m = m0 + mo + i * 16 + quad * 4 + reg;
+                    int n = n0 + no + j * 16 + r;
+                    if (mode) gpre1[(size_t)m * 256 + n] = acc[i][j][reg];
+                    else cat2b[(size_t)m * 512 + n] = (u16)f2bf(acc[i][j][reg]);
+                }
+    } else {
+        int l = bx - 512;
+        int n0 = (l & 3) * 64, m0 = (l >> 2) * 64;
+        mfma_core(cat2b_ssd, 512, wbf + WB_GATE + 256, 512, m0, n0, 256, As, Ws, acc, tid);
+        #pragma unroll
+        for (int i = 0; i < 2; i++)
+            #pragma unroll
+            for (int j = 0; j < 2; j++)
+                #pragma unroll
+                for (int reg = 0; reg < 4; reg++) {
+                    int m = m0 + mo + i * 16 + quad * 4 + reg;
+                    int n = n0 + no + j * 16 + r;
+                    gpre2[(size_t)m * 256 + n] = acc[i][j][reg];
+                }
     }
+}
+
+__global__ __launch_bounds__(256) void final_k(const float* __restrict__ gpre1,
+                                               const float* __restrict__ gpre2,
+                                               const float* __restrict__ gate_b,
+                                               const u16* __restrict__ cat2b,
+                                               const float* __restrict__ x,
+                                               float* __restrict__ outp) {
+    int idx4 = (blockIdx.x * 256 + threadIdx.x) * 4;
+    int m = idx4 >> 8, n = idx4 & 255;
+    float4 g1 = *(const float4*)(gpre1 + (size_t)m * 256 + n);
+    float4 g2 = *(const float4*)(gpre2 + (size_t)m * 256 + n);
+    float4 gb = *(const float4*)(gate_b + n);
+    s4v sm = *(const s4v*)(cat2b + (size_t)m * 512 + n);
+    s4v sd = *(const s4v*)(cat2b + (size_t)m * 512 + 256 + n);
+    float4 xv = *(const float4*)(x + (size_t)m * 256 + n);
+    float4 o;
+    float gv[4] = {g1.x + g2.x + gb.x, g1.y + g2.y + gb.y,
+                   g1.z + g2.z + gb.z, g1.w + g2.w + gb.w};
+    float xr[4] = {xv.x, xv.y, xv.z, xv.w};
+    float* op = (float*)&o;
     #pragma unroll
-    for (int i = 0; i < 2; i++)
-        #pragma unroll
-        for (int j = 0; j < 2; j++)
-            #pragma unroll
-            for (int reg = 0; reg < 4; reg++) {
-                int m = m0 + mo + i * 16 + quad * 4 + reg;
-                int n = n0 + no + j * 16 + r;
-                cat2b[(size_t)m * 512 + n] = (u16)f2bf(acc[i][j][reg]);
-            }
-}
-
-__global__ __launch_bounds__(256) void gate_gemm(const u16* __restrict__ cat2b,
-                                                 const u16* __restrict__ w_gate,
-                                                 const float* __restrict__ gate_b,
-                                                 const float* __restrict__ xres,
-                                                 float* __restrict__ fout) {
-    __shared__ u16 As[64][40];
-    __shared__ u16 Ws[64][40];
-    int tid = threadIdx.x;
-    int wave = tid >> 6, lane = tid & 63;
-    int quad = lane >> 4, r = lane & 15;
-    int m0 = blockIdx.y * 64, n0 = blockIdx.x * 64;
-    int mo = (wave >> 1) * 32, no = (wave & 1) * 32;
-    f4v acc[2][2];
-    #pragma unroll
-    for (int i = 0; i < 2; i++)
-        #pragma unroll
-        for (int j = 0; j < 2; j++) acc[i][j] = (f4v){0.f, 0.f, 0.f, 0.f};
-    for (int k0 = 0; k0 < 512; k0 += 32) {
-        {
-            int m = tid >> 2, kk = (tid & 3) * 8;
-            *(s8v*)&As[m][kk] = *(const s8v*)(cat2b + (size_t)(m0 + m) * 512 + k0 + kk);
-        }
-        {
-            int n = tid >> 2, kk = (tid & 3) * 8;
-            *(s8v*)&Ws[n][kk] = *(const s8v*)(w_gate + (size_t)(n0 + n) * 512 + k0 + kk);
-        }
-        __syncthreads();
-        s8v af[2], bf[2];
-        #pragma unroll
-        for (int i = 0; i < 2; i++) af[i] = *(const s8v*)&As[mo + i * 16 + r][quad * 8];
-        #pragma unroll
-        for (int j = 0; j < 2; j++) bf[j] = *(const s8v*)&Ws[no + j * 16 + r][quad * 8];
-        #pragma unroll
-        for (int i = 0; i < 2; i++)
-            #pragma unroll
-            for (int j = 0; j < 2; j++)
-                acc[i][j] = __builtin_amdgcn_mfma_f32_16x16x32_bf16(af[i], bf[j], acc[i][j], 0, 0, 0);
-        __syncthreads();
+    for (int i = 0; i < 4; i++) {
+        float gg = 1.0f / (1.0f + __expf(-gv[i]));
+        float ssm = bf2f((u16)sm[i]);
+        float ssd = bf2f((u16)sd[i]);
+        op[i] = xr[i] + gg * ssm + (1.0f - gg) * ssd;
     }
-    #pragma unroll
-    for (int i = 0; i < 2; i++)
-        #pragma unroll
-        for (int j = 0; j < 2; j++)
-            #pragma unroll
-            for (int reg = 0; reg < 4; reg++) {
-                int m = m0 + mo + i * 16 + quad * 4 + reg;
-                int n = n0 + no + j * 16 + r;
-                float v = acc[i][j][reg] + gate_b[n];
-                float gg = 1.0f / (1.0f + __expf(-v));
-                float ssm = bf2f(cat2b[(size_t)m * 512 + n]);
-                float ssd = bf2f(cat2b[(size_t)m * 512 + 256 + n]);
-                fout[(size_t)m * 256 + n] = xres[(size_t)m * 256 + n] + gg * ssm + (1.0f - gg) * ssd;
-            }
+    *(float4*)(outp + (size_t)m * 256 + n) = o;
 }
 
 extern "C" void kernel_launch(void* const* d_in, const int* in_sizes, int n_in,
@@ -886,7 +859,7 @@
     float* zT    = ws + off; off += (size_t)DIm * M;
     float* xcT   = ws + off; off += (size_t)DIm * M;
     float* dtmT  = ws + off; off += (size_t)DIm * M;
-    float* dbc   = ws + off; off += (size_t)M * 144;
+    float* dbc2  = ws + off; off += (size_t)M * 128;
     float* qbuf  = ws + off; off += (size_t)M * Dm;
     float* kmat  = ws + off; off += (size_t)M * Dm;
     float* vmat  = ws + off; off += (size_t)M * Dm;
@@ -894,6 +867,8 @@
     float* hloc  = ws + off; off += (size_t)NCH * NCHK * Ssz;
     float* Pc    = ws + off; off += (size_t)NCH * NCHK * Ssz;
     float* kvtot = ws + off; off += (size_t)64 * 256;
+    float* gpre1 = ws + off; off += (size_t)M * Dm;
+    float* gpre2 = ws + off; off += (size_t)M * Dm;
     u16* ub = (u16*)(ws + off);
     size_t uo = 0;
     u16* xnb  = ub + uo; uo += (size_t)M * Dm;
@@ -908,30 +883,28 @@
     u16* attnb= ub + uo; uo += (size_t)M * Dm;
     u16* cat2b= ub + uo; uo += (size_t)M * 2 * Dm;
     u16* yTb  = ub + uo; uo += (size_t)DIm * M;
-    u16* wbf  = ub + uo; uo += 1318912;
+    u16* wbf  = ub + uo; uo += 1843200;
     u16* xcb  = cat2b;
 
-    ln_pool<<<1156, 256, 0, stream>>>(x, ln_g, ln_b, xnb, xd2b, xd4b, xd8b,
-        in_proj_w, k_w, v_w, mq_w, fuse_w, x_proj_w, out_w, o_w, gate_w, wbf);
-
-    proj8<<<2016, 256, 0, stream>>>(xnb, xd2b, xd4b, xd8b, wbf,
+    ln_pool<<<1476, 256, 0, stream>>>(x, ln_g, ln_b, xnb, xd2b, xd4b, xd8b,
+        in_proj_w, k_w, v_w, mq_w, fuse_w, x_proj_w, out_w, o_w, gate_w, dt_w, wbf);
+
+    proj8<<<2048, 256, 0, stream>>>(xnb, xd2b, xd4b, xd8b, wbf,
         k_b, v_b, mq_b, xmb, zT, kmat, vmat, q0b, qd2b, qd4b, qd8b);
 
-    mid2<<<768, 256, 0, stream>>>(q0b, qd2b, qd4b, qd8b, wbf + 655360, fuse_b, qbuf,
+    mid2<<<768, 256, 0, stream>>>(q0b, qd2b, qd4b, qd8b, wbf + WB_FUSE, fuse_b, qbuf,
         xmb, conv_w, conv_b, xcb, xcT);
 
-    xproj_ap1<<<1216, 256, 0, stream>>>(xcb, wbf + 917504, dbc, kmat, vmat, log_tau, loc);
-
-    dt_ap2<<<576, 256, 0, stream>>>(dbc, dt_w, dt_b, dtmT, loc, log_tau, kvtot);
-
-    sp1_ap3<<<9216, 256, 0, stream>>>(xcT, dtmT, dbc, A_log, hloc, Pc,
-        qbuf, kmat, vmat, log_tau, loc, kvtot, attnb);
-
-    comb_ssd<<<768, 256, 0, stream>>>(hloc, Pc, attnb, wbf + 1122304, o_b, cat2b);
-
-    scan_pass3<<<8192, 256, 0, stream>>>(xcT, dtmT, zT, dbc, A_log, D_ssm, hloc, yTb);
-
-    outg<<<256, 256, 0, stream>>>(yTb, wbf + 991232, cat2b);
-
-    gate_gemm<<<dim3(4, 64), 256, 0, stream>>>(cat2b, wbf + 1187840, gate_b, x, outp);
-}
+    xproj_ap1<<<1664, 256, 0, stream>>>(xcb, wbf, dbc2, dt_b, dtmT, kmat, vmat, log_tau, loc);
+
+    sp1_ap2<<<8256, 256, 0, stream>>>(xcT, dtmT, dbc2, A_log, hloc, Pc, loc, log_tau, kvtot);
+
+    comb_ap3<<<1536, 256, 0, stream>>>(hloc, Pc, qbuf, kmat, vmat, log_tau, loc, kvtot, attnb);
+
+    p3_og<<<8448, 256, 0, stream>>>(xcT, dtmT, zT, dbc2, A_log, D_ssm, hloc, yTb,
+        attnb, wbf + WB_O, o_b, cat2b);
+
+    outg_gpre<<<768, 256, 0, stream>>>(yTb, wbf, cat2b + 256, cat2b, gpre1, gpre2);
+
+    final_k<<<1024, 256, 0, stream>>>(gpre1, gpre2, gate_b, cat2b, x, outp);
+}
```

Measured after the change: 316.8 us. +7.7%, slower.
